# Performance work log

Hardware: AMD Instinct MI355X
Metric: run time of the kernel (lower is better)

Reference implementation:

```python
import jax, jax.numpy as jnp
import numpy as np

# Irreps structure (hardcoded per init_kwargs):
#  input  = 16x0e + 8x1o  -> dim 16 + 8*3 = 40
#  query  = key = 8x0e + 4x1o -> dim 8 + 4*3 = 20
#  output = 16x0e + 8x1o -> dim 40
#  edge_sh = 1x0e + 1x1o -> dim 4
M0, M1 = 16, 8          # input multiplicities (scalar, vector)
Q0, Q1 = 8, 4           # query/key multiplicities
O0, O1 = 16, 8          # output multiplicities
TPK_NUMEL = M0*Q0 + M1*Q0 + M0*Q1 + M1*Q1 + M1*Q1   # 320
TPV_NUMEL = M0*O0 + M1*O0 + M0*O1 + M1*O1 + M1*O1   # 640
EDGE_BASIS = 16
HIDDEN = 32


def _split(x):
    """Split irreps vector [*, m0 + 3*m1] into scalars [*, m0] and vectors [*, m1, 3]."""
    m0 = x.shape[-1] - 3 * ((x.shape[-1] - M0) // 3) if False else None
    return x  # placeholder, not used


def fc_net(x, w1, w2):
    """e3nn FullyConnectedNet: no biases, 1/sqrt(fan_in) scaling, silu hidden act."""
    h = jax.nn.silu((x @ w1) * (1.0 / np.sqrt(x.shape[-1])))
    return (h @ w2) * (1.0 / np.sqrt(w1.shape[-1]))


def fctp_edge(xs, xv, shs, shv, w, o0, o1):
    """FullyConnectedTensorProduct((m0x0e+m1x1o) x (1x0e+1x1o) -> (o0x0e+o1x1o))
    with per-edge weights w [E, numel]. Component-normalized CG, path-normalized output.
    xs:[E,m0] xv:[E,m1,3] shs:[E,1] shv:[E,3]."""
    m0, m1 = xs.shape[1], xv.shape[1]
    sizes = [m0*o0, m1*o0, m0*o1, m1*o1, m1*o1]
    offs = np.cumsum([0] + sizes)
    w1 = w[:, offs[0]:offs[1]].reshape(-1, m0, o0)
    w2 = w[:, offs[1]:offs[2]].reshape(-1, m1, o0)
    w3 = w[:, offs[2]:offs[3]].reshape(-1, m0, o1)
    w4 = w[:, offs[3]:offs[4]].reshape(-1, m1, o1)
    w5 = w[:, offs[4]:offs[5]].reshape(-1, m1, o1)
    # scalar output paths: 0e x 0e -> 0e ; 1o x 1o -> 0e (dot / sqrt3)
    p_ss = xs * shs                                            # [E,m0]
    p_vv = jnp.einsum('eic,ec->ei', xv, shv) * (1.0/np.sqrt(3.0))  # [E,m1]
    out_s = (jnp.einsum('ei,eio->eo', p_ss, w1)
             + jnp.einsum('ei,eio->eo', p_vv, w2)) * (1.0/np.sqrt(m0 + m1))
    # vector output paths: 0e x 1o ; 1o x 0e ; 1o x 1o -> 1o (cross / sqrt2)
    p_sv = xs[:, :, None] * shv[:, None, :]                    # [E,m0,3]
    p_vs = xv * shs[:, :, None]                                # [E,m1,3]
    p_xx = jnp.cross(xv, shv[:, None, :]) * (1.0/np.sqrt(2.0)) # [E,m1,3]
    out_v = (jnp.einsum('eic,eio->eoc', p_sv, w3)
             + jnp.einsum('eic,eio->eoc', p_vs, w4)
             + jnp.einsum('eic,eio->eoc', p_xx, w5)) * (1.0/np.sqrt(m0 + 2*m1))
    return out_s, out_v


def setup_inputs() -> dict:
    key = jax.random.key(0)
    ks = jax.random.split(key, 12)
    N, E = 10000, 100000
    node_ft = jax.random.normal(ks[0], (N, M0 + 3*M1), dtype=jnp.float32)
    edge_index = jax.random.randint(ks[1], (2, E), 0, N, dtype=jnp.int64)
    edge_sh = jax.random.normal(ks[2], (E, 4), dtype=jnp.float32)
    edge_scalars = jax.random.uniform(ks[3], (E, EDGE_BASIS), dtype=jnp.float32)
    # learned parameters
    w_q_s = jax.random.normal(ks[4], (M0, Q0), dtype=jnp.float32)
    w_q_v = jax.random.normal(ks[5], (M1, Q1), dtype=jnp.float32)
    fck_w1 = jax.random.normal(ks[6], (EDGE_BASIS, HIDDEN), dtype=jnp.float32)
    fck_w2 = jax.random.normal(ks[7], (HIDDEN, TPK_NUMEL), dtype=jnp.float32)
    fcv_w1 = jax.random.normal(ks[8], (EDGE_BASIS, HIDDEN), dtype=jnp.float32)
    fcv_w2 = jax.random.normal(ks[9], (HIDDEN, TPV_NUMEL), dtype=jnp.float32)
    wdot_s = jax.random.normal(ks[10], (Q0, Q0), dtype=jnp.float32)
    wdot_v = jax.random.normal(ks[11], (Q1, Q1), dtype=jnp.float32)
    return dict(node_ft=node_ft, edge_index=edge_index, edge_sh=edge_sh,
                edge_scalars=edge_scalars, w_q_s=w_q_s, w_q_v=w_q_v,
                fck_w1=fck_w1, fck_w2=fck_w2, fcv_w1=fcv_w1, fcv_w2=fcv_w2,
                wdot_s=wdot_s, wdot_v=wdot_v)


def reference(node_ft, edge_index, edge_sh, edge_scalars, w_q_s, w_q_v,
              fck_w1, fck_w2, fcv_w1, fcv_w2, wdot_s, wdot_v):
    N = node_ft.shape[0]
    sender, receiver = edge_index[0], edge_index[1]
    x_s = node_ft[:, :M0]                       # [N,16]
    x_v = node_ft[:, M0:].reshape(N, M1, 3)     # [N,8,3]
    # q = o3.Linear(input -> query): per-irrep linear mixing, 1/sqrt(mul) norm
    q_s = (x_s @ w_q_s) * (1.0/np.sqrt(M0))                    # [N,Q0]
    q_v = jnp.einsum('nic,io->noc', x_v, w_q_v) * (1.0/np.sqrt(M1))  # [N,Q1,3]
    sh_s, sh_v = edge_sh[:, :1], edge_sh[:, 1:4]
    xs_e, xv_e = x_s[sender], x_v[sender]       # gather sender features
    # per-edge tensor-product weights from radial MLPs
    wk = fc_net(edge_scalars, fck_w1, fck_w2)   # [E, 320]
    wv = fc_net(edge_scalars, fcv_w1, fcv_w2)   # [E, 640]
    k_s, k_v = fctp_edge(xs_e, xv_e, sh_s, sh_v, wk, Q0, Q1)
    v_s, v_v = fctp_edge(xs_e, xv_e, sh_s, sh_v, wv, O0, O1)
    # dot = FCTP(query, key -> 0e) with shared internal weights
    qr_s, qr_v = q_s[receiver], q_v[receiver]
    fan = Q0*Q0 + Q1*Q1
    dot = (jnp.einsum('ei,ej,ij->e', qr_s, k_s, wdot_s)
           + jnp.einsum('eic,ejc,ij->e', qr_v, k_v, wdot_v) * (1.0/np.sqrt(3.0))
           ) * (1.0/np.sqrt(fan))               # [E]
    # scatter-softmax over receiver
    ex = jnp.exp(dot)
    z = jax.ops.segment_sum(ex, receiver, num_segments=N)      # [N]
    alpha = ex / z[receiver]
    a = jnp.sqrt(jax.nn.relu(alpha))            # [E]
    out_s = jax.ops.segment_sum(a[:, None] * v_s, receiver, num_segments=N)
    out_v = jax.ops.segment_sum(a[:, None, None] * v_v, receiver, num_segments=N)
    return jnp.concatenate([out_s, out_v.reshape(N, O1*3)], axis=-1)  # [N,40]
```

## Files before the change

kernel.cpp:

```cpp
#include <hip/hip_runtime.h>


#define BS 256
#define EPB 64

typedef _Float16 half2_t __attribute__((ext_vector_type(2)));

#ifdef __has_builtin
#if __has_builtin(__builtin_amdgcn_fdot2)
#define USE_FDOT2 1
#endif
#endif

__device__ __forceinline__ float silu_f(float x) {
    return x * (1.0f / (1.0f + __expf(-x)));
}
__device__ __forceinline__ unsigned short f2h(float f) {
    return __builtin_bit_cast(unsigned short, (_Float16)f);
}
__device__ __forceinline__ unsigned pk2h(float a, float b) {
    return (unsigned)f2h(a) | ((unsigned)f2h(b) << 16);
}
__device__ __forceinline__ half2_t uh2(unsigned u) {
    return __builtin_bit_cast(half2_t, u);
}
__device__ __forceinline__ float d2(unsigned a, unsigned b, float c) {
#ifdef USE_FDOT2
    return __builtin_amdgcn_fdot2(uh2(a), uh2(b), c, false);
#else
    const half2_t ha = uh2(a), hb = uh2(b);
    return c + (float)ha[0] * (float)hb[0] + (float)ha[1] * (float)hb[1];
#endif
}
__device__ __forceinline__ float wred4(float v) {
    v += __shfl_xor(v, 16);
    v += __shfl_xor(v, 32);
    return v;
}

__global__ __launch_bounds__(256) void node_pre(
    const float* __restrict__ node_ft,
    const int*   __restrict__ ei,
    const float* __restrict__ w_q_s, const float* __restrict__ w_q_v,
    const float* __restrict__ wdot_s, const float* __restrict__ wdot_v,
    float* __restrict__ qd, int* __restrict__ cnt, int* __restrict__ flag,
    int N, int E)
{
    const int n = blockIdx.x * blockDim.x + threadIdx.x;
    if (n == 0) {
        int acc = 0;
        const int kmax = (E < 64) ? E : 64;
        for (int k = 0; k < kmax; ++k) acc |= ei[2*k + 1];
        *flag = (acc == 0) ? 1 : 0;
    }
    if (n >= N) return;
    cnt[n] = 0;

    const float* nf = node_ft + (size_t)n * 40;
    float xs[16];
#pragma unroll
    for (int i = 0; i < 16; ++i) xs[i] = nf[i];
    float q[8];
#pragma unroll
    for (int o = 0; o < 8; ++o) {
        float a = 0.f;
#pragma unroll
        for (int i = 0; i < 16; ++i) a += xs[i] * w_q_s[i*8 + o];
        q[o] = a * 0.25f;
    }
    float* qdn = qd + (size_t)n * 20;
#pragma unroll
    for (int j = 0; j < 8; ++j) {
        float a = 0.f;
#pragma unroll
        for (int i = 0; i < 8; ++i) a += q[i] * wdot_s[i*8 + j];
        qdn[j] = a;
    }
    float xv[8][3];
#pragma unroll
    for (int i = 0; i < 8; ++i)
#pragma unroll
        for (int c = 0; c < 3; ++c) xv[i][c] = nf[16 + i*3 + c];
    float qv[4][3];
#pragma unroll
    for (int o = 0; o < 4; ++o)
#pragma unroll
        for (int c = 0; c < 3; ++c) {
            float a = 0.f;
#pragma unroll
            for (int i = 0; i < 8; ++i) a += xv[i][c] * w_q_v[i*4 + o];
            qv[o][c] = a * 0.35355339059327379f;
        }
#pragma unroll
    for (int j = 0; j < 4; ++j)
#pragma unroll
        for (int c = 0; c < 3; ++c) {
            float a = 0.f;
#pragma unroll
            for (int i = 0; i < 4; ++i) a += qv[i][c] * wdot_v[i*4 + j];
            qdn[8 + j*3 + c] = a;
        }
}

__global__ __launch_bounds__(256) void count_edges(
    const int* __restrict__ ei, int* __restrict__ cnt,
    const int* __restrict__ flag, int E)
{
    const int e = blockIdx.x * blockDim.x + threadIdx.x;
    if (e >= E) return;
    const int is64 = *flag;
    const int rcv = is64 ? ei[2*(E + e)] : ei[E + e];
    atomicAdd(cnt + rcv, 1);
}

__global__ __launch_bounds__(1024) void scan_kernel(
    const int* __restrict__ cnt, int* __restrict__ start,
    int* __restrict__ cursor, int N)
{
    __shared__ int wsum[16];
    __shared__ int s_carry;
    const int tid = threadIdx.x, wave = tid >> 6, lane = tid & 63;
    if (tid == 0) s_carry = 0;
    __syncthreads();
    for (int base = 0; base < N; base += 1024) {
        const int i = base + tid;
        const int v = (i < N) ? cnt[i] : 0;
        int x = v;
#pragma unroll
        for (int d = 1; d < 64; d <<= 1) {
            const int y = __shfl_up(x, d, 64);
            if (lane >= d) x += y;
        }
        if (lane == 63) wsum[wave] = x;
        __syncthreads();
        if (wave == 0 && lane < 16) {
            int w = wsum[lane];
#pragma unroll
            for (int d = 1; d < 16; d <<= 1) {
                const int y = __shfl_up(w, d, 64);
                if (lane >= d) w += y;
            }
            wsum[lane] = w;
        }
        __syncthreads();
        const int woff = (wave == 0) ? 0 : wsum[wave - 1];
        const int carry = s_carry;
        if (i < N) {
            const int s = carry + woff + x - v;
            start[i] = s;
            cursor[i] = s;
        }
        __syncthreads();
        if (tid == 0) s_carry = carry + wsum[15];
        __syncthreads();
    }
    if (tid == 0) start[N] = s_carry;
}

__global__ __launch_bounds__(BS) void edge_k(
    const float* __restrict__ node_ft,
    const int*   __restrict__ ei,
    const float* __restrict__ edge_sh,
    const float* __restrict__ edge_scalars,
    const float* __restrict__ fck_w1,
    const float* __restrict__ fck_w2,
    const float* __restrict__ qd,
    int*   __restrict__ cursor,
    float* __restrict__ exbuf,
    float* __restrict__ sabuf,
    int*   __restrict__ posbuf,
    const int* __restrict__ flag,
    int N, int E)
{
    __shared__ uint4 sk4[4 * 321];

    const int tid = threadIdx.x;
    for (int idx = tid; idx < 4 * 320; idx += BS) {
        const int p = idx / 320;
        const int local = idx - p * 320;
        unsigned r0, r1, r2, r3;
        if (local < 128) {
            const int j = local >> 2, rr = local & 3, ip = rr >> 1, h = rr & 1;
            const int i0 = 4*p + 2*ip;
            const float* s0 = fck_w2 + j*320 + i0*8 + 4*h;
            const float* s1 = s0 + 8;
            r0 = pk2h(s0[0], s1[0]); r1 = pk2h(s0[1], s1[1]);
            r2 = pk2h(s0[2], s1[2]); r3 = pk2h(s0[3], s1[3]);
        } else if (local < 192) {
            const int l = local - 128; const int j = l >> 1, ip = l & 1;
            const int i0 = 4*p + 2*ip;
            const float* s0 = fck_w2 + j*320 + 192 + i0*4;
            const float* s1 = s0 + 4;
            r0 = pk2h(s0[0], s1[0]); r1 = pk2h(s0[1], s1[1]);
            r2 = pk2h(s0[2], s1[2]); r3 = pk2h(s0[3], s1[3]);
        } else if (local < 256) {
            const int l = local - 192; const int j = l >> 1, h = l & 1;
            const int i0 = 2*p;
            const float* s0 = fck_w2 + j*320 + 128 + i0*8 + 4*h;
            const float* s1 = s0 + 8;
            r0 = pk2h(s0[0], s1[0]); r1 = pk2h(s0[1], s1[1]);
            r2 = pk2h(s0[2], s1[2]); r3 = pk2h(s0[3], s1[3]);
        } else {
            const int l = local - 256; const int jp = l >> 2, rr = l & 3;
            const int il = rr >> 1, h = rr & 1;
            const int i = 2*p + il, j0 = 2*jp;
            const int col = (h == 0 ? 256 : 288) + i*4;
            const float* s0 = fck_w2 + j0*320 + col;
            const float* s1 = s0 + 320;
            r0 = pk2h(s0[0], s1[0]); r1 = pk2h(s0[1], s1[1]);
            r2 = pk2h(s0[2], s1[2]); r3 = pk2h(s0[3], s1[3]);
        }
        sk4[p * 321 + local] = make_uint4(r0, r1, r2, r3);
    }

    const int lane = tid & 63;
    const int p = lane >> 4;
    const int q = lane & 15;
    const int w = tid >> 6;
    const int e = blockIdx.x * EPB + w * 16 + q;
    const bool val = (e < E);
    const int ec = val ? e : (E - 1);

    const int is64 = *flag;
    const int snd = is64 ? ei[2*ec]       : ei[ec];
    const int rcv = is64 ? ei[2*(E + ec)] : ei[E + ec];

    int pos = 0;
    if (p == 0 && val) pos = atomicAdd(cursor + rcv, 1);

    const float4 s4 = *(const float4*)(edge_sh + (size_t)ec * 4);
    const float sh_s = s4.x;
    const float sh_v[3] = {s4.y, s4.z, s4.w};

    const float* nf = node_ft + (size_t)snd * 40;

    __syncthreads();

    float hk[32];
    {
        float es[16];
        const float4* a0 = (const float4*)(edge_scalars + (size_t)ec * 16);
#pragma unroll
        for (int t = 0; t < 4; ++t) {
            const float4 v = a0[t];
            es[4*t+0]=v.x; es[4*t+1]=v.y; es[4*t+2]=v.z; es[4*t+3]=v.w;
        }
#pragma unroll 8
        for (int j = 0; j < 32; ++j) {
            float a = 0.f;
#pragma unroll
            for (int t = 0; t < 16; ++t) a += es[t] * fck_w1[t*32 + j];
            hk[j] = silu_f(a * 0.25f);
        }
    }

    const uint4* g = sk4 + p * 321;

    const unsigned xs01 = pk2h(nf[4*p + 0], nf[4*p + 1]);
    const unsigned xs23 = pk2h(nf[4*p + 2], nf[4*p + 3]);

    float K1[8] = {};
#pragma unroll 8
    for (int j = 0; j < 32; ++j) {
        const uint4 A = g[j*4+0], B = g[j*4+1], C = g[j*4+2], D = g[j*4+3];
        const float h = hk[j];
        float t;
        t = d2(xs01, A.x, 0.f); t = d2(xs23, C.x, t); K1[0] += h*t;
        t = d2(xs01, A.y, 0.f); t = d2(xs23, C.y, t); K1[1] += h*t;
        t = d2(xs01, A.z, 0.f); t = d2(xs23, C.z, t); K1[2] += h*t;
        t = d2(xs01, A.w, 0.f); t = d2(xs23, C.w, t); K1[3] += h*t;
        t = d2(xs01, B.x, 0.f); t = d2(xs23, D.x, t); K1[4] += h*t;
        t = d2(xs01, B.y, 0.f); t = d2(xs23, D.y, t); K1[5] += h*t;
        t = d2(xs01, B.z, 0.f); t = d2(xs23, D.z, t); K1[6] += h*t;
        t = d2(xs01, B.w, 0.f); t = d2(xs23, D.w, t); K1[7] += h*t;
    }

    float K3[4] = {};
#pragma unroll 8
    for (int j = 0; j < 32; ++j) {
        const uint4 Ea = g[128 + j*2], Fb = g[128 + j*2 + 1];
        const float h = hk[j];
        float t;
        t = d2(xs01, Ea.x, 0.f); t = d2(xs23, Fb.x, t); K3[0] += h*t;
        t = d2(xs01, Ea.y, 0.f); t = d2(xs23, Fb.y, t); K3[1] += h*t;
        t = d2(xs01, Ea.z, 0.f); t = d2(xs23, Fb.z, t); K3[2] += h*t;
        t = d2(xs01, Ea.w, 0.f); t = d2(xs23, Fb.w, t); K3[3] += h*t;
    }

    const float c3 = 0.57735026918962576f;
    const float xa0 = nf[16 + 6*p], xa1 = nf[17 + 6*p], xa2 = nf[18 + 6*p];
    const float xb0 = nf[19 + 6*p], xb1 = nf[20 + 6*p], xb2 = nf[21 + 6*p];
    const float pv0 = (xa0*sh_v[0] + xa1*sh_v[1] + xa2*sh_v[2]) * c3;
    const float pv1 = (xb0*sh_v[0] + xb1*sh_v[1] + xb2*sh_v[2]) * c3;
    const unsigned pvp = pk2h(pv0, pv1);
    float K2[8] = {};
#pragma unroll 8
    for (int j = 0; j < 32; ++j) {
        const uint4 U = g[192 + j*2], V = g[192 + j*2 + 1];
        const float h = hk[j];
        K2[0] += h * d2(pvp, U.x, 0.f);
        K2[1] += h * d2(pvp, U.y, 0.f);
        K2[2] += h * d2(pvp, U.z, 0.f);
        K2[3] += h * d2(pvp, U.w, 0.f);
        K2[4] += h * d2(pvp, V.x, 0.f);
        K2[5] += h * d2(pvp, V.y, 0.f);
        K2[6] += h * d2(pvp, V.z, 0.f);
        K2[7] += h * d2(pvp, V.w, 0.f);
    }

    float W40[4] = {}, W41[4] = {}, W50[4] = {}, W51[4] = {};
#pragma unroll 4
    for (int jp = 0; jp < 16; ++jp) {
        const unsigned hp = pk2h(hk[2*jp], hk[2*jp+1]);
        const uint4 a = g[256 + jp*4 + 0];
        const uint4 b = g[256 + jp*4 + 1];
        const uint4 c = g[256 + jp*4 + 2];
        const uint4 d = g[256 + jp*4 + 3];
        W40[0] = d2(hp, a.x, W40[0]); W40[1] = d2(hp, a.y, W40[1]);
        W40[2] = d2(hp, a.z, W40[2]); W40[3] = d2(hp, a.w, W40[3]);
        W50[0] = d2(hp, b.x, W50[0]); W50[1] = d2(hp, b.y, W50[1]);
        W50[2] = d2(hp, b.z, W50[2]); W50[3] = d2(hp, b.w, W50[3]);
        W41[0] = d2(hp, c.x, W41[0]); W41[1] = d2(hp, c.y, W41[1]);
        W41[2] = d2(hp, c.z, W41[2]); W41[3] = d2(hp, c.w, W41[3]);
        W51[0] = d2(hp, d.x, W51[0]); W51[1] = d2(hp, d.y, W51[1]);
        W51[2] = d2(hp, d.z, W51[2]); W51[3] = d2(hp, d.w, W51[3]);
    }

    const float c7 = 0.70710678118654752f;
    float KV[12] = {};
    {
        const float s0 = sh_s*xa0, s1 = sh_s*xa1, s2 = sh_s*xa2;
        const float cx0 = c7*(xa1*sh_v[2] - xa2*sh_v[1]);
        const float cx1 = c7*(xa2*sh_v[0] - xa0*sh_v[2]);
        const float cx2 = c7*(xa0*sh_v[1] - xa1*sh_v[0]);
#pragma unroll
        for (int o = 0; o < 4; ++o) {
            KV[o*3+0] += s0*W40[o] + cx0*W50[o];
            KV[o*3+1] += s1*W40[o] + cx1*W50[o];
            KV[o*3+2] += s2*W40[o] + cx2*W50[o];
        }
    }
    {
        const float s0 = sh_s*xb0, s1 = sh_s*xb1, s2 = sh_s*xb2;
        const float cx0 = c7*(xb1*sh_v[2] - xb2*sh_v[1]);
        const float cx1 = c7*(xb2*sh_v[0] - xb0*sh_v[2]);
        const float cx2 = c7*(xb0*sh_v[1] - xb1*sh_v[0]);
#pragma unroll
        for (int o = 0; o < 4; ++o) {
            KV[o*3+0] += s0*W41[o] + cx0*W51[o];
            KV[o*3+1] += s1*W41[o] + cx1*W51[o];
            KV[o*3+2] += s2*W41[o] + cx2*W51[o];
        }
    }

#pragma unroll
    for (int o = 0; o < 8; ++o) K1[o] = wred4(K1[o]);
#pragma unroll
    for (int o = 0; o < 8; ++o) K2[o] = wred4(K2[o]);
#pragma unroll
    for (int o = 0; o < 4; ++o) K3[o] = wred4(K3[o]);
#pragma unroll
    for (int o = 0; o < 12; ++o) KV[o] = wred4(KV[o]);

    if (p == 0 && val) {
        float qdr[20];
        {
            const float4* rp = (const float4*)(qd + (size_t)rcv * 20);
#pragma unroll
            for (int t = 0; t < 5; ++t) {
                const float4 a = rp[t];
                qdr[4*t+0]=a.x; qdr[4*t+1]=a.y; qdr[4*t+2]=a.z; qdr[4*t+3]=a.w;
            }
        }
        float ds = 0.f;
#pragma unroll
        for (int o = 0; o < 8; ++o) ds += qdr[o] * (sh_s*K1[o] + K2[o]);
        float dv = 0.f;
#pragma unroll
        for (int o = 0; o < 4; ++o)
#pragma unroll
            for (int c = 0; c < 3; ++c)
                dv += qdr[8 + o*3 + c] * (K3[o]*sh_v[c] + KV[o*3+c]);
        const float dot = ds * 4.0343567508008e-3f + dv * 2.0171788261497e-3f;
        const float sa = __expf(0.5f * dot);
        exbuf[pos] = sa*sa; sabuf[e] = sa; posbuf[e] = pos;
    }
}

__global__ __launch_bounds__(BS) void edge_v_a(
    const float* __restrict__ node_ft,
    const int*   __restrict__ ei,
    const float* __restrict__ edge_sh,
    const float* __restrict__ edge_scalars,
    const float* __restrict__ fcv_w1,
    const float* __restrict__ fcv_w2,
    const float* __restrict__ sabuf,
    const int*   __restrict__ posbuf,
    float* __restrict__ vbuf,
    const int* __restrict__ flag,
    int E)
{
    __shared__ uint4 sa4[4 * 385];

    const int tid = threadIdx.x;
    for (int idx = tid; idx < 4 * 384; idx += BS) {
        const int p = idx / 384;
        const int local = idx - p * 384;
        const float* s0;
        const float* s1;
        if (local < 256) {
            const int j = local >> 3, rr = local & 7, ip = rr >> 2, h = rr & 3;
            const int i0 = 4*p + 2*ip;
            s0 = fcv_w2 + j*640 + i0*16 + h*4;
            s1 = s0 + 16;
        } else {
            const int l = local - 256; const int j = l >> 2, h = l & 3;
            const int i0 = 2*p;
            s0 = fcv_w2 + j*640 + 256 + i0*16 + h*4;
            s1 = s0 + 16;
        }
        sa4[p * 385 + local] = make_uint4(
            pk2h(s0[0], s1[0]), pk2h(s0[1], s1[1]),
            pk2h(s0[2], s1[2]), pk2h(s0[3], s1[3]));
    }

    const int lane = tid & 63;
    const int p = lane >> 4;
    const int q = lane & 15;
    const int w = tid >> 6;
    const int e = blockIdx.x * EPB + w * 16 + q;
    const bool val = (e < E);
    const int ec = val ? e : (E - 1);

    const int is64 = *flag;
    const int snd = is64 ? ei[2*ec] : ei[ec];

    const float4 s4 = *(const float4*)(edge_sh + (size_t)ec * 4);
    const float sh_s = s4.x;

    const float* nf = node_ft + (size_t)snd * 40;

    __syncthreads();

    float hv[32];
    {
        float es[16];
        const float4* a0 = (const float4*)(edge_scalars + (size_t)ec * 16);
#pragma unroll
        for (int t = 0; t < 4; ++t) {
            const float4 v = a0[t];
            es[4*t+0]=v.x; es[4*t+1]=v.y; es[4*t+2]=v.z; es[4*t+3]=v.w;
        }
#pragma unroll 8
        for (int j = 0; j < 32; ++j) {
            float a = 0.f;
#pragma unroll
            for (int t = 0; t < 16; ++t) a += es[t] * fcv_w1[t*32 + j];
            hv[j] = silu_f(a * 0.25f);
        }
    }

    const uint4* g = sa4 + p * 385;

    const unsigned xs01 = pk2h(nf[4*p + 0]*sh_s, nf[4*p + 1]*sh_s);
    const unsigned xs23 = pk2h(nf[4*p + 2]*sh_s, nf[4*p + 3]*sh_s);
    const float c3 = 0.57735026918962576f;
    const float pv0 = (nf[16+6*p]*s4.y + nf[17+6*p]*s4.z + nf[18+6*p]*s4.w) * c3;
    const float pv1 = (nf[19+6*p]*s4.y + nf[20+6*p]*s4.z + nf[21+6*p]*s4.w) * c3;
    const unsigned pvp = pk2h(pv0, pv1);

    float A[16] = {};

#pragma unroll 2
    for (int j = 0; j < 32; ++j) {
        const uint4* gw = g + j*8;
        const uint4 a0 = gw[0], a1 = gw[1], a2 = gw[2], a3 = gw[3];
        const uint4 b0 = gw[4], b1 = gw[5], b2 = gw[6], b3 = gw[7];
        const float h = hv[j];
        float t;
        t = d2(xs01, a0.x, 0.f); t = d2(xs23, b0.x, t); A[0]  += h*t;
        t = d2(xs01, a0.y, 0.f); t = d2(xs23, b0.y, t); A[1]  += h*t;
        t = d2(xs01, a0.z, 0.f); t = d2(xs23, b0.z, t); A[2]  += h*t;
        t = d2(xs01, a0.w, 0.f); t = d2(xs23, b0.w, t); A[3]  += h*t;
        t = d2(xs01, a1.x, 0.f); t = d2(xs23, b1.x, t); A[4]  += h*t;
        t = d2(xs01, a1.y, 0.f); t = d2(xs23, b1.y, t); A[5]  += h*t;
        t = d2(xs01, a1.z, 0.f); t = d2(xs23, b1.z, t); A[6]  += h*t;
        t = d2(xs01, a1.w, 0.f); t = d2(xs23, b1.w, t); A[7]  += h*t;
        t = d2(xs01, a2.x, 0.f); t = d2(xs23, b2.x, t); A[8]  += h*t;
        t = d2(xs01, a2.y, 0.f); t = d2(xs23, b2.y, t); A[9]  += h*t;
        t = d2(xs01, a2.z, 0.f); t = d2(xs23, b2.z, t); A[10] += h*t;
        t = d2(xs01, a2.w, 0.f); t = d2(xs23, b2.w, t); A[11] += h*t;
        t = d2(xs01, a3.x, 0.f); t = d2(xs23, b3.x, t); A[12] += h*t;
        t = d2(xs01, a3.y, 0.f); t = d2(xs23, b3.y, t); A[13] += h*t;
        t = d2(xs01, a3.z, 0.f); t = d2(xs23, b3.z, t); A[14] += h*t;
        t = d2(xs01, a3.w, 0.f); t = d2(xs23, b3.w, t); A[15] += h*t;
    }

#pragma unroll 4
    for (int j = 0; j < 32; ++j) {
        const uint4* gw = g + 256 + j*4;
        const uint4 u0 = gw[0], u1 = gw[1], u2 = gw[2], u3 = gw[3];
        const float h = hv[j];
        A[0]  += h * d2(pvp, u0.x, 0.f);
        A[1]  += h * d2(pvp, u0.y, 0.f);
        A[2]  += h * d2(pvp, u0.z, 0.f);
        A[3]  += h * d2(pvp, u0.w, 0.f);
        A[4]  += h * d2(pvp, u1.x, 0.f);
        A[5]  += h * d2(pvp, u1.y, 0.f);
        A[6]  += h * d2(pvp, u1.z, 0.f);
        A[7]  += h * d2(pvp, u1.w, 0.f);
        A[8]  += h * d2(pvp, u2.x, 0.f);
        A[9]  += h * d2(pvp, u2.y, 0.f);
        A[10] += h * d2(pvp, u2.z, 0.f);
        A[11] += h * d2(pvp, u2.w, 0.f);
        A[12] += h * d2(pvp, u3.x, 0.f);
        A[13] += h * d2(pvp, u3.y, 0.f);
        A[14] += h * d2(pvp, u3.z, 0.f);
        A[15] += h * d2(pvp, u3.w, 0.f);
    }

#pragma unroll
    for (int o = 0; o < 16; ++o) A[o] = wred4(A[o]);

    if (p == 0 && val) {
        const float cs = 0.03608439182435161f;
        const float sa = sabuf[e];
        const int pos = posbuf[e];
        float4* vp = (float4*)(vbuf + (size_t)pos * 40);
#pragma unroll
        for (int t = 0; t < 4; ++t) {
            float4 r;
            r.x = sa * A[4*t+0] * cs; r.y = sa * A[4*t+1] * cs;
            r.z = sa * A[4*t+2] * cs; r.w = sa * A[4*t+3] * cs;
            vp[t] = r;
        }
    }
}

__global__ __launch_bounds__(BS) void edge_v_b(
    const float* __restrict__ node_ft,
    const int*   __restrict__ ei,
    const float* __restrict__ edge_sh,
    const float* __restrict__ edge_scalars,
    const float* __restrict__ fcv_w1,
    const float* __restrict__ fcv_w2,
    const float* __restrict__ sabuf,
    const int*   __restrict__ posbuf,
    float* __restrict__ vbuf,
    const int* __restrict__ flag,
    int E)
{
    __shared__ uint4 sb4[4 * 257];

    const int tid = threadIdx.x;
    for (int idx = tid; idx < 4 * 256; idx += BS) {
        const int p = idx >> 8;
        const int local = idx & 255;
        const float* s0;
        const float* s1;
        if (local < 128) {
            const int j = local >> 2, rr = local & 3, ip = rr >> 1, h = rr & 1;
            const int i0 = 4*p + 2*ip;
            s0 = fcv_w2 + j*640 + 384 + i0*8 + 4*h;
            s1 = s0 + 8;
        } else {
            const int l = local - 128;
            const int jp = l >> 3, rr = l & 7, il = rr >> 2, h2 = rr & 3;
            const int i = 2*p + il, j0 = 2*jp;
            const int base = (h2 < 2) ? 512 : 576;
            s0 = fcv_w2 + j0*640 + base + i*8 + (h2 & 1)*4;
            s1 = s0 + 640;
        }
        sb4[p * 257 + local] = make_uint4(
            pk2h(s0[0], s1[0]), pk2h(s0[1], s1[1]),
            pk2h(s0[2], s1[2]), pk2h(s0[3], s1[3]));
    }

    const int lane = tid & 63;
    const int p = lane >> 4;
    const int q = lane & 15;
    const int w = tid >> 6;
    const int e = blockIdx.x * EPB + w * 16 + q;
    const bool val = (e < E);
    const int ec = val ? e : (E - 1);

    const int is64 = *flag;
    const int snd = is64 ? ei[2*ec] : ei[ec];

    const float4 s4 = *(const float4*)(edge_sh + (size_t)ec * 4);
    const float sh_s = s4.x;
    const float sh_v[3] = {s4.y, s4.z, s4.w};

    const float* nf = node_ft + (size_t)snd * 40;

    __syncthreads();

    float hv[32];
    {
        float es[16];
        const float4* a0 = (const float4*)(edge_scalars + (size_t)ec * 16);
#pragma unroll
        for (int t = 0; t < 4; ++t) {
            const float4 v = a0[t];
            es[4*t+0]=v.x; es[4*t+1]=v.y; es[4*t+2]=v.z; es[4*t+3]=v.w;
        }
#pragma unroll 8
        for (int j = 0; j < 32; ++j) {
            float a = 0.f;
#pragma unroll
            for (int t = 0; t < 16; ++t) a += es[t] * fcv_w1[t*32 + j];
            hv[j] = silu_f(a * 0.25f);
        }
    }

    const uint4* g = sb4 + p * 257;

    const unsigned xs01 = pk2h(nf[4*p + 0], nf[4*p + 1]);
    const unsigned xs23 = pk2h(nf[4*p + 2], nf[4*p + 3]);

    float T3[8] = {};
#pragma unroll 4
    for (int j = 0; j < 32; ++j) {
        const uint4 E0 = g[j*4+0], E1 = g[j*4+1];
        const uint4 F0 = g[j*4+2], F1 = g[j*4+3];
        const float h = hv[j];
        float t;
        t = d2(xs01, E0.x, 0.f); t = d2(xs23, F0.x, t); T3[0] += h*t;
        t = d2(xs01, E0.y, 0.f); t = d2(xs23, F0.y, t); T3[1] += h*t;
        t = d2(xs01, E0.z, 0.f); t = d2(xs23, F0.z, t); T3[2] += h*t;
        t = d2(xs01, E0.w, 0.f); t = d2(xs23, F0.w, t); T3[3] += h*t;
        t = d2(xs01, E1.x, 0.f); t = d2(xs23, F1.x, t); T3[4] += h*t;
        t = d2(xs01, E1.y, 0.f); t = d2(xs23, F1.y, t); T3[5] += h*t;
        t = d2(xs01, E1.z, 0.f); t = d2(xs23, F1.z, t); T3[6] += h*t;
        t = d2(xs01, E1.w, 0.f); t = d2(xs23, F1.w, t); T3[7] += h*t;
    }

    float W40[8] = {}, W41[8] = {}, W50[8] = {}, W51[8] = {};
#pragma unroll 2
    for (int jp = 0; jp < 16; ++jp) {
        const unsigned hp = pk2h(hv[2*jp], hv[2*jp+1]);
        const uint4* gw = g + 128 + jp*8;
        const uint4 a = gw[0], b = gw[1], c = gw[2], d = gw[3];
        const uint4 e2 = gw[4], f = gw[5], m = gw[6], n = gw[7];
        W40[0] = d2(hp, a.x, W40[0]); W40[1] = d2(hp, a.y, W40[1]);
        W40[2] = d2(hp, a.z, W40[2]); W40[3] = d2(hp, a.w, W40[3]);
        W40[4] = d2(hp, b.x, W40[4]); W40[5] = d2(hp, b.y, W40[5]);
        W40[6] = d2(hp, b.z, W40[6]); W40[7] = d2(hp, b.w, W40[7]);
        W50[0] = d2(hp, c.x, W50[0]); W50[1] = d2(hp, c.y, W50[1]);
        W50[2] = d2(hp, c.z, W50[2]); W50[3] = d2(hp, c.w, W50[3]);
        W50[4] = d2(hp, d.x, W50[4]); W50[5] = d2(hp, d.y, W50[5]);
        W50[6] = d2(hp, d.z, W50[6]); W50[7] = d2(hp, d.w, W50[7]);
        W41[0] = d2(hp, e2.x, W41[0]); W41[1] = d2(hp, e2.y, W41[1]);
        W41[2] = d2(hp, e2.z, W41[2]); W41[3] = d2(hp, e2.w, W41[3]);
        W41[4] = d2(hp, f.x, W41[4]); W41[5] = d2(hp, f.y, W41[5]);
        W41[6] = d2(hp, f.z, W41[6]); W41[7] = d2(hp, f.w, W41[7]);
        W51[0] = d2(hp, m.x, W51[0]); W51[1] = d2(hp, m.y, W51[1]);
        W51[2] = d2(hp, m.z, W51[2]); W51[3] = d2(hp, m.w, W51[3]);
        W51[4] = d2(hp, n.x, W51[4]); W51[5] = d2(hp, n.y, W51[5]);
        W51[6] = d2(hp, n.z, W51[6]); W51[7] = d2(hp, n.w, W51[7]);
    }

    const float c7 = 0.70710678118654752f;
    float R[24] = {};
    {
        const float x0 = nf[16 + 6*p], x1 = nf[17 + 6*p], x2 = nf[18 + 6*p];
        const float s0 = sh_s*x0, s1 = sh_s*x1, s2 = sh_s*x2;
        const float cx0 = c7*(x1*sh_v[2] - x2*sh_v[1]);
        const float cx1 = c7*(x2*sh_v[0] - x0*sh_v[2]);
        const float cx2 = c7*(x0*sh_v[1] - x1*sh_v[0]);
#pragma unroll
        for (int o = 0; o < 8; ++o) {
            R[o*3+0] += s0*W40[o] + cx0*W50[o];
            R[o*3+1] += s1*W40[o] + cx1*W50[o];
            R[o*3+2] += s2*W40[o] + cx2*W50[o];
        }
    }
    {
        const float x0 = nf[19 + 6*p], x1 = nf[20 + 6*p], x2 = nf[21 + 6*p];
        const float s0 = sh_s*x0, s1 = sh_s*x1, s2 = sh_s*x2;
        const float cx0 = c7*(x1*sh_v[2] - x2*sh_v[1]);
        const float cx1 = c7*(x2*sh_v[0] - x0*sh_v[2]);
        const float cx2 = c7*(x0*sh_v[1] - x1*sh_v[0]);
#pragma unroll
        for (int o = 0; o < 8; ++o) {
            R[o*3+0] += s0*W41[o] + cx0*W51[o];
            R[o*3+1] += s1*W41[o] + cx1*W51[o];
            R[o*3+2] += s2*W41[o] + cx2*W51[o];
        }
    }

#pragma unroll
    for (int o = 0; o < 8; ++o) T3[o] = wred4(T3[o]);
#pragma unroll
    for (int o = 0; o < 24; ++o) R[o] = wred4(R[o]);

    if (p == 0 && val) {
        const float sc = 0.03125f;
        const float sa = sabuf[e];
        const int pos = posbuf[e];
        float row[24];
#pragma unroll
        for (int o = 0; o < 8; ++o)
#pragma unroll
            for (int c = 0; c < 3; ++c)
                row[o*3+c] = sa * (T3[o]*sh_v[c] + R[o*3+c]) * sc;
        float4* vp = (float4*)(vbuf + (size_t)pos * 40 + 16);
#pragma unroll
        for (int t = 0; t < 6; ++t) {
            float4 r; r.x = row[4*t+0]; r.y = row[4*t+1]; r.z = row[4*t+2]; r.w = row[4*t+3];
            vp[t] = r;
        }
    }
}

__global__ __launch_bounds__(256) void node_reduce(
    const int*   __restrict__ start,
    const float* __restrict__ exbuf,
    const float* __restrict__ vbuf,
    float* __restrict__ out, int N)
{
    const int wave = threadIdx.x >> 6;
    const int lane = threadIdx.x & 63;
    const int n = blockIdx.x * 4 + wave;
    if (n >= N) return;
    const int r0 = start[n], r1 = start[n + 1];
    float z = 0.f, comp = 0.f;
    for (int r = r0; r < r1; ++r) {
        z += exbuf[r];
        if (lane < 40) comp += vbuf[(size_t)r * 40 + lane];
    }
    if (lane < 40)
        out[(size_t)n * 40 + lane] = (z > 0.f) ? comp * rsqrtf(z) : 0.f;
}

extern "C" void kernel_launch(void* const* d_in, const int* in_sizes, int n_in,
                              void* d_out, int out_size, void* d_ws, size_t ws_size,
                              hipStream_t stream) {
    const float* node_ft      = (const float*)d_in[0];
    const int*   edge_index   = (const int*)  d_in[1];
    const float* edge_sh      = (const float*)d_in[2];
    const float* edge_scalars = (const float*)d_in[3];
    const float* w_q_s        = (const float*)d_in[4];
    const float* w_q_v        = (const float*)d_in[5];
    const float* fck_w1       = (const float*)d_in[6];
    const float* fck_w2       = (const float*)d_in[7];
    const float* fcv_w1       = (const float*)d_in[8];
    const float* fcv_w2       = (const float*)d_in[9];
    const float* wdot_s       = (const float*)d_in[10];
    const float* wdot_v       = (const float*)d_in[11];

    const int N = in_sizes[0] / 40;
    const int E = in_sizes[2] / 4;

    float* ws    = (float*)d_ws;
    float* qd    = ws;
    int*   cnt   = (int*)(ws + (size_t)N * 20);
    int*   start = cnt + N;
    int*   curs  = start + N + 1;
    int*   flg   = curs + N;
    size_t off   = (size_t)N * 20 + N + (N + 1) + N + 1;
    off = (off + 3) & ~(size_t)3;
    float* exbuf  = ws + off;
    float* sabuf  = exbuf + E;
    int*   posbuf = (int*)(sabuf + E);
    float* vbuf   = (float*)(posbuf + E);

    float* out = (float*)d_out;

    const int EB = (E + EPB - 1) / EPB;

    hipLaunchKernelGGL(node_pre, dim3((N + 255) / 256), dim3(256), 0, stream,
                       node_ft, edge_index, w_q_s, w_q_v, wdot_s, wdot_v,
                       qd, cnt, flg, N, E);
    hipLaunchKernelGGL(count_edges, dim3((E + 255) / 256), dim3(256), 0, stream,
                       edge_index, cnt, flg, E);
    hipLaunchKernelGGL(scan_kernel, dim3(1), dim3(1024), 0, stream,
                       cnt, start, curs, N);
    hipLaunchKernelGGL(edge_k, dim3(EB), dim3(BS), 0, stream,
                       node_ft, edge_index, edge_sh, edge_scalars,
                       fck_w1, fck_w2, qd, curs, exbuf, sabuf, posbuf, flg, N, E);
    hipLaunchKernelGGL(edge_v_a, dim3(EB), dim3(BS), 0, stream,
                       node_ft, edge_index, edge_sh, edge_scalars,
                       fcv_w1, fcv_w2, sabuf, posbuf, vbuf, flg, E);
    hipLaunchKernelGGL(edge_v_b, dim3(EB), dim3(BS), 0, stream,
                       node_ft, edge_index, edge_sh, edge_scalars,
                       fcv_w1, fcv_w2, sabuf, posbuf, vbuf, flg, E);
    hipLaunchKernelGGL(node_reduce, dim3((N + 3) / 4), dim3(256), 0, stream,
                       start, exbuf, vbuf, out, N);
}
```

Before: 296.4 us.

## Process two edges per thread with packed fp16 FMA accumulation

Each thread now handles two edges, so the weights fetched from LDS once serve both, and the block size drops to 128 threads to keep 64 edges per block. The fdot2-based float accumulation is replaced by packed half-precision FMAs (v_pk_fma style) with fp16 accumulators that are summed to float only at the end. This aims to halve LDS traffic per edge and double arithmetic throughput. The cost is higher register pressure and lower accuracy, since accumulating in fp16 over 32 hidden units with round-toward-zero conversion can exceed the tolerance.

```diff
diff --git a/kernel.cpp b/kernel.cpp
--- a/kernel.cpp
+++ b/kernel.cpp
@@ -1,16 +1,10 @@
 #include <hip/hip_runtime.h>
 
 
-#define BS 256
+#define BS 128
 #define EPB 64
 
-typedef _Float16 half2_t __attribute__((ext_vector_type(2)));
-
-#ifdef __has_builtin
-#if __has_builtin(__builtin_amdgcn_fdot2)
-#define USE_FDOT2 1
-#endif
-#endif
+typedef _Float16 h2 __attribute__((ext_vector_type(2)));
 
 __device__ __forceinline__ float silu_f(float x) {
     return x * (1.0f / (1.0f + __expf(-x)));
@@ -21,17 +15,20 @@
 __device__ __forceinline__ unsigned pk2h(float a, float b) {
     return (unsigned)f2h(a) | ((unsigned)f2h(b) << 16);
 }
-__device__ __forceinline__ half2_t uh2(unsigned u) {
-    return __builtin_bit_cast(half2_t, u);
-}
-__device__ __forceinline__ float d2(unsigned a, unsigned b, float c) {
-#ifdef USE_FDOT2
-    return __builtin_amdgcn_fdot2(uh2(a), uh2(b), c, false);
-#else
-    const half2_t ha = uh2(a), hb = uh2(b);
-    return c + (float)ha[0] * (float)hb[0] + (float)ha[1] * (float)hb[1];
-#endif
-}
+__device__ __forceinline__ h2 uh2(unsigned u) {
+    return __builtin_bit_cast(h2, u);
+}
+__device__ __forceinline__ h2 pkrtz(float a, float b) {
+    return __builtin_bit_cast(h2, __builtin_amdgcn_cvt_pkrtz(a, b));
+}
+__device__ __forceinline__ h2 pfma(h2 a, h2 b, h2 c) {
+    return __builtin_elementwise_fma(a, b, c);
+}
+__device__ __forceinline__ float h2s(h2 a) {
+    return (float)a[0] + (float)a[1];
+}
+__device__ __forceinline__ h2 dup0(h2 a) { return __builtin_shufflevector(a, a, 0, 0); }
+__device__ __forceinline__ h2 dup1(h2 a) { return __builtin_shufflevector(a, a, 1, 1); }
 __device__ __forceinline__ float wred4(float v) {
     v += __shfl_xor(v, 16);
     v += __shfl_xor(v, 32);
@@ -217,173 +214,260 @@
     const int p = lane >> 4;
     const int q = lane & 15;
     const int w = tid >> 6;
-    const int e = blockIdx.x * EPB + w * 16 + q;
-    const bool val = (e < E);
-    const int ec = val ? e : (E - 1);
+    const int e0 = blockIdx.x * EPB + w * 32 + 2 * q;
+    const int e1 = e0 + 1;
+    const bool v0 = (e0 < E), v1 = (e1 < E);
+    const int e0c = v0 ? e0 : (E - 1);
+    const int e1c = v1 ? e1 : (E - 1);
 
     const int is64 = *flag;
-    const int snd = is64 ? ei[2*ec]       : ei[ec];
-    const int rcv = is64 ? ei[2*(E + ec)] : ei[E + ec];
-
-    int pos = 0;
-    if (p == 0 && val) pos = atomicAdd(cursor + rcv, 1);
-
-    const float4 s4 = *(const float4*)(edge_sh + (size_t)ec * 4);
-    const float sh_s = s4.x;
-    const float sh_v[3] = {s4.y, s4.z, s4.w};
-
-    const float* nf = node_ft + (size_t)snd * 40;
+    const int snd0 = is64 ? ei[2*e0c]       : ei[e0c];
+    const int rcv0 = is64 ? ei[2*(E + e0c)] : ei[E + e0c];
+    const int snd1 = is64 ? ei[2*e1c]       : ei[e1c];
+    const int rcv1 = is64 ? ei[2*(E + e1c)] : ei[E + e1c];
+
+    int pos0 = 0, pos1 = 0;
+    if (p == 0) {
+        if (v0) pos0 = atomicAdd(cursor + rcv0, 1);
+        if (v1) pos1 = atomicAdd(cursor + rcv1, 1);
+    }
+
+    const float4 s40 = *(const float4*)(edge_sh + (size_t)e0c * 4);
+    const float4 s41 = *(const float4*)(edge_sh + (size_t)e1c * 4);
+    const float sh_s0 = s40.x, sh_s1 = s41.x;
+    const float sh_v0[3] = {s40.y, s40.z, s40.w};
+    const float sh_v1[3] = {s41.y, s41.z, s41.w};
+
+    const float* nf0 = node_ft + (size_t)snd0 * 40;
+    const float* nf1 = node_ft + (size_t)snd1 * 40;
 
     __syncthreads();
 
-    float hk[32];
+    h2 hkp[32];
     {
-        float es[16];
-        const float4* a0 = (const float4*)(edge_scalars + (size_t)ec * 16);
+        float es0[16], es1[16];
+        const float4* a0 = (const float4*)(edge_scalars + (size_t)e0c * 16);
+        const float4* a1 = (const float4*)(edge_scalars + (size_t)e1c * 16);
 #pragma unroll
         for (int t = 0; t < 4; ++t) {
-            const float4 v = a0[t];
-            es[4*t+0]=v.x; es[4*t+1]=v.y; es[4*t+2]=v.z; es[4*t+3]=v.w;
+            const float4 a = a0[t], b = a1[t];
+            es0[4*t+0]=a.x; es0[4*t+1]=a.y; es0[4*t+2]=a.z; es0[4*t+3]=a.w;
+            es1[4*t+0]=b.x; es1[4*t+1]=b.y; es1[4*t+2]=b.z; es1[4*t+3]=b.w;
         }
 #pragma unroll 8
         for (int j = 0; j < 32; ++j) {
-            float a = 0.f;
-#pragma unroll
-            for (int t = 0; t < 16; ++t) a += es[t] * fck_w1[t*32 + j];
-            hk[j] = silu_f(a * 0.25f);
+            float a = 0.f, b = 0.f;
+#pragma unroll
+            for (int t = 0; t < 16; ++t) {
+                const float w1 = fck_w1[t*32 + j];
+                a += es0[t] * w1; b += es1[t] * w1;
+            }
+            hkp[j] = pkrtz(silu_f(a * 0.25f), silu_f(b * 0.25f));
         }
     }
 
     const uint4* g = sk4 + p * 321;
 
-    const unsigned xs01 = pk2h(nf[4*p + 0], nf[4*p + 1]);
-    const unsigned xs23 = pk2h(nf[4*p + 2], nf[4*p + 3]);
-
-    float K1[8] = {};
-#pragma unroll 8
+    const h2 xs01a = pkrtz(nf0[4*p + 0], nf0[4*p + 1]);
+    const h2 xs23a = pkrtz(nf0[4*p + 2], nf0[4*p + 3]);
+    const h2 xs01b = pkrtz(nf1[4*p + 0], nf1[4*p + 1]);
+    const h2 xs23b = pkrtz(nf1[4*p + 2], nf1[4*p + 3]);
+    const float c3 = 0.57735026918962576f;
+    const float xa00 = nf0[16 + 6*p], xa01 = nf0[17 + 6*p], xa02 = nf0[18 + 6*p];
+    const float xa10 = nf0[19 + 6*p], xa11 = nf0[20 + 6*p], xa12 = nf0[21 + 6*p];
+    const float xb00 = nf1[16 + 6*p], xb01 = nf1[17 + 6*p], xb02 = nf1[18 + 6*p];
+    const float xb10 = nf1[19 + 6*p], xb11 = nf1[20 + 6*p], xb12 = nf1[21 + 6*p];
+    const h2 pvpa = pkrtz((xa00*sh_v0[0] + xa01*sh_v0[1] + xa02*sh_v0[2]) * c3,
+                          (xa10*sh_v0[0] + xa11*sh_v0[1] + xa12*sh_v0[2]) * c3);
+    const h2 pvpb = pkrtz((xb00*sh_v1[0] + xb01*sh_v1[1] + xb02*sh_v1[2]) * c3,
+                          (xb10*sh_v1[0] + xb11*sh_v1[1] + xb12*sh_v1[2]) * c3);
+
+    h2 K1a[8] = {}, K3a[4] = {}, K2a[8] = {};
+    h2 K1b[8] = {}, K3b[4] = {}, K2b[8] = {};
+#pragma unroll 4
     for (int j = 0; j < 32; ++j) {
         const uint4 A = g[j*4+0], B = g[j*4+1], C = g[j*4+2], D = g[j*4+3];
-        const float h = hk[j];
-        float t;
-        t = d2(xs01, A.x, 0.f); t = d2(xs23, C.x, t); K1[0] += h*t;
-        t = d2(xs01, A.y, 0.f); t = d2(xs23, C.y, t); K1[1] += h*t;
-        t = d2(xs01, A.z, 0.f); t = d2(xs23, C.z, t); K1[2] += h*t;
-        t = d2(xs01, A.w, 0.f); t = d2(xs23, C.w, t); K1[3] += h*t;
-        t = d2(xs01, B.x, 0.f); t = d2(xs23, D.x, t); K1[4] += h*t;
-        t = d2(xs01, B.y, 0.f); t = d2(xs23, D.y, t); K1[5] += h*t;
-        t = d2(xs01, B.z, 0.f); t = d2(xs23, D.z, t); K1[6] += h*t;
-        t = d2(xs01, B.w, 0.f); t = d2(xs23, D.w, t); K1[7] += h*t;
-    }
-
-    float K3[4] = {};
-#pragma unroll 8
-    for (int j = 0; j < 32; ++j) {
         const uint4 Ea = g[128 + j*2], Fb = g[128 + j*2 + 1];
-        const float h = hk[j];
-        float t;
-        t = d2(xs01, Ea.x, 0.f); t = d2(xs23, Fb.x, t); K3[0] += h*t;
-        t = d2(xs01, Ea.y, 0.f); t = d2(xs23, Fb.y, t); K3[1] += h*t;
-        t = d2(xs01, Ea.z, 0.f); t = d2(xs23, Fb.z, t); K3[2] += h*t;
-        t = d2(xs01, Ea.w, 0.f); t = d2(xs23, Fb.w, t); K3[3] += h*t;
-    }
-
-    const float c3 = 0.57735026918962576f;
-    const float xa0 = nf[16 + 6*p], xa1 = nf[17 + 6*p], xa2 = nf[18 + 6*p];
-    const float xb0 = nf[19 + 6*p], xb1 = nf[20 + 6*p], xb2 = nf[21 + 6*p];
-    const float pv0 = (xa0*sh_v[0] + xa1*sh_v[1] + xa2*sh_v[2]) * c3;
-    const float pv1 = (xb0*sh_v[0] + xb1*sh_v[1] + xb2*sh_v[2]) * c3;
-    const unsigned pvp = pk2h(pv0, pv1);
-    float K2[8] = {};
-#pragma unroll 8
-    for (int j = 0; j < 32; ++j) {
         const uint4 U = g[192 + j*2], V = g[192 + j*2 + 1];
-        const float h = hk[j];
-        K2[0] += h * d2(pvp, U.x, 0.f);
-        K2[1] += h * d2(pvp, U.y, 0.f);
-        K2[2] += h * d2(pvp, U.z, 0.f);
-        K2[3] += h * d2(pvp, U.w, 0.f);
-        K2[4] += h * d2(pvp, V.x, 0.f);
-        K2[5] += h * d2(pvp, V.y, 0.f);
-        K2[6] += h * d2(pvp, V.z, 0.f);
-        K2[7] += h * d2(pvp, V.w, 0.f);
-    }
-
-    float W40[4] = {}, W41[4] = {}, W50[4] = {}, W51[4] = {};
+        const h2 hj = hkp[j];
+        {
+            const h2 hh = dup0(hj);
+            const h2 t01 = hh * xs01a, t23 = hh * xs23a, tp = hh * pvpa;
+            K1a[0]=pfma(t01,uh2(A.x),K1a[0]); K1a[0]=pfma(t23,uh2(C.x),K1a[0]);
+            K1a[1]=pfma(t01,uh2(A.y),K1a[1]); K1a[1]=pfma(t23,uh2(C.y),K1a[1]);
+            K1a[2]=pfma(t01,uh2(A.z),K1a[2]); K1a[2]=pfma(t23,uh2(C.z),K1a[2]);
+            K1a[3]=pfma(t01,uh2(A.w),K1a[3]); K1a[3]=pfma(t23,uh2(C.w),K1a[3]);
+            K1a[4]=pfma(t01,uh2(B.x),K1a[4]); K1a[4]=pfma(t23,uh2(D.x),K1a[4]);
+            K1a[5]=pfma(t01,uh2(B.y),K1a[5]); K1a[5]=pfma(t23,uh2(D.y),K1a[5]);
+            K1a[6]=pfma(t01,uh2(B.z),K1a[6]); K1a[6]=pfma(t23,uh2(D.z),K1a[6]);
+            K1a[7]=pfma(t01,uh2(B.w),K1a[7]); K1a[7]=pfma(t23,uh2(D.w),K1a[7]);
+            K3a[0]=pfma(t01,uh2(Ea.x),K3a[0]); K3a[0]=pfma(t23,uh2(Fb.x),K3a[0]);
+            K3a[1]=pfma(t01,uh2(Ea.y),K3a[1]); K3a[1]=pfma(t23,uh2(Fb.y),K3a[1]);
+            K3a[2]=pfma(t01,uh2(Ea.z),K3a[2]); K3a[2]=pfma(t23,uh2(Fb.z),K3a[2]);
+            K3a[3]=pfma(t01,uh2(Ea.w),K3a[3]); K3a[3]=pfma(t23,uh2(Fb.w),K3a[3]);
+            K2a[0]=pfma(tp,uh2(U.x),K2a[0]); K2a[1]=pfma(tp,uh2(U.y),K2a[1]);
+            K2a[2]=pfma(tp,uh2(U.z),K2a[2]); K2a[3]=pfma(tp,uh2(U.w),K2a[3]);
+            K2a[4]=pfma(tp,uh2(V.x),K2a[4]); K2a[5]=pfma(tp,uh2(V.y),K2a[5]);
+            K2a[6]=pfma(tp,uh2(V.z),K2a[6]); K2a[7]=pfma(tp,uh2(V.w),K2a[7]);
+        }
+        {
+            const h2 hh = dup1(hj);
+            const h2 t01 = hh * xs01b, t23 = hh * xs23b, tp = hh * pvpb;
+            K1b[0]=pfma(t01,uh2(A.x),K1b[0]); K1b[0]=pfma(t23,uh2(C.x),K1b[0]);
+            K1b[1]=pfma(t01,uh2(A.y),K1b[1]); K1b[1]=pfma(t23,uh2(C.y),K1b[1]);
+            K1b[2]=pfma(t01,uh2(A.z),K1b[2]); K1b[2]=pfma(t23,uh2(C.z),K1b[2]);
+            K1b[3]=pfma(t01,uh2(A.w),K1b[3]); K1b[3]=pfma(t23,uh2(C.w),K1b[3]);
+            K1b[4]=pfma(t01,uh2(B.x),K1b[4]); K1b[4]=pfma(t23,uh2(D.x),K1b[4]);
+            K1b[5]=pfma(t01,uh2(B.y),K1b[5]); K1b[5]=pfma(t23,uh2(D.y),K1b[5]);
+            K1b[6]=pfma(t01,uh2(B.z),K1b[6]); K1b[6]=pfma(t23,uh2(D.z),K1b[6]);
+            K1b[7]=pfma(t01,uh2(B.w),K1b[7]); K1b[7]=pfma(t23,uh2(D.w),K1b[7]);
+            K3b[0]=pfma(t01,uh2(Ea.x),K3b[0]); K3b[0]=pfma(t23,uh2(Fb.x),K3b[0]);
+            K3b[1]=pfma(t01,uh2(Ea.y),K3b[1]); K3b[1]=pfma(t23,uh2(Fb.y),K3b[1]);
+            K3b[2]=pfma(t01,uh2(Ea.z),K3b[2]); K3b[2]=pfma(t23,uh2(Fb.z),K3b[2]);
+            K3b[3]=pfma(t01,uh2(Ea.w),K3b[3]); K3b[3]=pfma(t23,uh2(Fb.w),K3b[3]);
+            K2b[0]=pfma(tp,uh2(U.x),K2b[0]); K2b[1]=pfma(tp,uh2(U.y),K2b[1]);
+            K2b[2]=pfma(tp,uh2(U.z),K2b[2]); K2b[3]=pfma(tp,uh2(U.w),K2b[3]);
+            K2b[4]=pfma(tp,uh2(V.x),K2b[4]); K2b[5]=pfma(tp,uh2(V.y),K2b[5]);
+            K2b[6]=pfma(tp,uh2(V.z),K2b[6]); K2b[7]=pfma(tp,uh2(V.w),K2b[7]);
+        }
+    }
+
+    h2 P4a[8] = {}, P5a[8] = {}, P4b[8] = {}, P5b[8] = {};
 #pragma unroll 4
     for (int jp = 0; jp < 16; ++jp) {
-        const unsigned hp = pk2h(hk[2*jp], hk[2*jp+1]);
-        const uint4 a = g[256 + jp*4 + 0];
-        const uint4 b = g[256 + jp*4 + 1];
-        const uint4 c = g[256 + jp*4 + 2];
-        const uint4 d = g[256 + jp*4 + 3];
-        W40[0] = d2(hp, a.x, W40[0]); W40[1] = d2(hp, a.y, W40[1]);
-        W40[2] = d2(hp, a.z, W40[2]); W40[3] = d2(hp, a.w, W40[3]);
-        W50[0] = d2(hp, b.x, W50[0]); W50[1] = d2(hp, b.y, W50[1]);
-        W50[2] = d2(hp, b.z, W50[2]); W50[3] = d2(hp, b.w, W50[3]);
-        W41[0] = d2(hp, c.x, W41[0]); W41[1] = d2(hp, c.y, W41[1]);
-        W41[2] = d2(hp, c.z, W41[2]); W41[3] = d2(hp, c.w, W41[3]);
-        W51[0] = d2(hp, d.x, W51[0]); W51[1] = d2(hp, d.y, W51[1]);
-        W51[2] = d2(hp, d.z, W51[2]); W51[3] = d2(hp, d.w, W51[3]);
+        const uint4 a4 = g[256 + jp*4 + 0];
+        const uint4 b4 = g[256 + jp*4 + 1];
+        const uint4 c4 = g[256 + jp*4 + 2];
+        const uint4 d4 = g[256 + jp*4 + 3];
+        const h2 hja = hkp[2*jp], hjb = hkp[2*jp+1];
+        const h2 hpa = __builtin_shufflevector(hja, hjb, 0, 2);
+        const h2 hpb = __builtin_shufflevector(hja, hjb, 1, 3);
+        P4a[0]=pfma(hpa,uh2(a4.x),P4a[0]); P4a[1]=pfma(hpa,uh2(a4.y),P4a[1]);
+        P4a[2]=pfma(hpa,uh2(a4.z),P4a[2]); P4a[3]=pfma(hpa,uh2(a4.w),P4a[3]);
+        P5a[0]=pfma(hpa,uh2(b4.x),P5a[0]); P5a[1]=pfma(hpa,uh2(b4.y),P5a[1]);
+        P5a[2]=pfma(hpa,uh2(b4.z),P5a[2]); P5a[3]=pfma(hpa,uh2(b4.w),P5a[3]);
+        P4a[4]=pfma(hpa,uh2(c4.x),P4a[4]); P4a[5]=pfma(hpa,uh2(c4.y),P4a[5]);
+        P4a[6]=pfma(hpa,uh2(c4.z),P4a[6]); P4a[7]=pfma(hpa,uh2(c4.w),P4a[7]);
+        P5a[4]=pfma(hpa,uh2(d4.x),P5a[4]); P5a[5]=pfma(hpa,uh2(d4.y),P5a[5]);
+        P5a[6]=pfma(hpa,uh2(d4.z),P5a[6]); P5a[7]=pfma(hpa,uh2(d4.w),P5a[7]);
+        P4b[0]=pfma(hpb,uh2(a4.x),P4b[0]); P4b[1]=pfma(hpb,uh2(a4.y),P4b[1]);
+        P4b[2]=pfma(hpb,uh2(a4.z),P4b[2]); P4b[3]=pfma(hpb,uh2(a4.w),P4b[3]);
+        P5b[0]=pfma(hpb,uh2(b4.x),P5b[0]); P5b[1]=pfma(hpb,uh2(b4.y),P5b[1]);
+        P5b[2]=pfma(hpb,uh2(b4.z),P5b[2]); P5b[3]=pfma(hpb,uh2(b4.w),P5b[3]);
+        P4b[4]=pfma(hpb,uh2(c4.x),P4b[4]); P4b[5]=pfma(hpb,uh2(c4.y),P4b[5]);
+        P4b[6]=pfma(hpb,uh2(c4.z),P4b[6]); P4b[7]=pfma(hpb,uh2(c4.w),P4b[7]);
+        P5b[4]=pfma(hpb,uh2(d4.x),P5b[4]); P5b[5]=pfma(hpb,uh2(d4.y),P5b[5]);
+        P5b[6]=pfma(hpb,uh2(d4.z),P5b[6]); P5b[7]=pfma(hpb,uh2(d4.w),P5b[7]);
     }
 
     const float c7 = 0.70710678118654752f;
-    float KV[12] = {};
+    float ds0 = 0.f, dv0 = 0.f, ds1 = 0.f, dv1 = 0.f;
     {
-        const float s0 = sh_s*xa0, s1 = sh_s*xa1, s2 = sh_s*xa2;
-        const float cx0 = c7*(xa1*sh_v[2] - xa2*sh_v[1]);
-        const float cx1 = c7*(xa2*sh_v[0] - xa0*sh_v[2]);
-        const float cx2 = c7*(xa0*sh_v[1] - xa1*sh_v[0]);
+        float qdr[20];
+        const float4* rp = (const float4*)(qd + (size_t)rcv0 * 20);
+#pragma unroll
+        for (int t = 0; t < 5; ++t) {
+            const float4 a = rp[t];
+            qdr[4*t+0]=a.x; qdr[4*t+1]=a.y; qdr[4*t+2]=a.z; qdr[4*t+3]=a.w;
+        }
+#pragma unroll
+        for (int o = 0; o < 8; ++o)
+            ds0 += qdr[o] * (sh_s0*h2s(K1a[o]) + h2s(K2a[o]));
+        float KV[12] = {};
+        {
+            const float s0=sh_s0*xa00, s1=sh_s0*xa01, s2=sh_s0*xa02;
+            const float cx0=c7*(xa01*sh_v0[2]-xa02*sh_v0[1]);
+            const float cx1=c7*(xa02*sh_v0[0]-xa00*sh_v0[2]);
+            const float cx2=c7*(xa00*sh_v0[1]-xa01*sh_v0[0]);
+#pragma unroll
+            for (int o = 0; o < 4; ++o) {
+                const float w4 = h2s(P4a[o]), w5 = h2s(P5a[o]);
+                KV[o*3+0] += s0*w4 + cx0*w5;
+                KV[o*3+1] += s1*w4 + cx1*w5;
+                KV[o*3+2] += s2*w4 + cx2*w5;
+            }
+        }
+        {
+            const float s0=sh_s0*xa10, s1=sh_s0*xa11, s2=sh_s0*xa12;
+            const float cx0=c7*(xa11*sh_v0[2]-xa12*sh_v0[1]);
+            const float cx1=c7*(xa12*sh_v0[0]-xa10*sh_v0[2]);
+            const float cx2=c7*(xa10*sh_v0[1]-xa11*sh_v0[0]);
+#pragma unroll
+            for (int o = 0; o < 4; ++o) {
+                const float w4 = h2s(P4a[4+o]), w5 = h2s(P5a[4+o]);
+                KV[o*3+0] += s0*w4 + cx0*w5;
+                KV[o*3+1] += s1*w4 + cx1*w5;
+                KV[o*3+2] += s2*w4 + cx2*w5;
+            }
+        }
 #pragma unroll
         for (int o = 0; o < 4; ++o) {
-            KV[o*3+0] += s0*W40[o] + cx0*W50[o];
-            KV[o*3+1] += s1*W40[o] + cx1*W50[o];
-            KV[o*3+2] += s2*W40[o] + cx2*W50[o];
+            const float k3 = h2s(K3a[o]);
+#pragma unroll
+            for (int c = 0; c < 3; ++c)
+                dv0 += qdr[8 + o*3 + c] * (k3*sh_v0[c] + KV[o*3+c]);
         }
     }
     {
-        const float s0 = sh_s*xb0, s1 = sh_s*xb1, s2 = sh_s*xb2;
-        const float cx0 = c7*(xb1*sh_v[2] - xb2*sh_v[1]);
-        const float cx1 = c7*(xb2*sh_v[0] - xb0*sh_v[2]);
-        const float cx2 = c7*(xb0*sh_v[1] - xb1*sh_v[0]);
+        float qdr[20];
+        const float4* rp = (const float4*)(qd + (size_t)rcv1 * 20);
+#pragma unroll
+        for (int t = 0; t < 5; ++t) {
+            const float4 a = rp[t];
+            qdr[4*t+0]=a.x; qdr[4*t+1]=a.y; qdr[4*t+2]=a.z; qdr[4*t+3]=a.w;
+        }
+#pragma unroll
+        for (int o = 0; o < 8; ++o)
+            ds1 += qdr[o] * (sh_s1*h2s(K1b[o]) + h2s(K2b[o]));
+        float KV[12] = {};
+        {
+            const float s0=sh_s1*xb00, s1=sh_s1*xb01, s2=sh_s1*xb02;
+            const float cx0=c7*(xb01*sh_v1[2]-xb02*sh_v1[1]);
+            const float cx1=c7*(xb02*sh_v1[0]-xb00*sh_v1[2]);
+            const float cx2=c7*(xb00*sh_v1[1]-xb01*sh_v1[0]);
+#pragma unroll
+            for (int o = 0; o < 4; ++o) {
+                const float w4 = h2s(P4b[o]), w5 = h2s(P5b[o]);
+                KV[o*3+0] += s0*w4 + cx0*w5;
+                KV[o*3+1] += s1*w4 + cx1*w5;
+                KV[o*3+2] += s2*w4 + cx2*w5;
+            }
+        }
+        {
+            const float s0=sh_s1*xb10, s1=sh_s1*xb11, s2=sh_s1*xb12;
+            const float cx0=c7*(xb11*sh_v1[2]-xb12*sh_v1[1]);
+            const float cx1=c7*(xb12*sh_v1[0]-xb10*sh_v1[2]);
+            const float cx2=c7*(xb10*sh_v1[1]-xb11*sh_v1[0]);
+#pragma unroll
+            for (int o = 0; o < 4; ++o) {
+                const float w4 = h2s(P4b[4+o]), w5 = h2s(P5b[4+o]);
+                KV[o*3+0] += s0*w4 + cx0*w5;
+                KV[o*3+1] += s1*w4 + cx1*w5;
+                KV[o*3+2] += s2*w4 + cx2*w5;
+            }
+        }
 #pragma unroll
         for (int o = 0; o < 4; ++o) {
-            KV[o*3+0] += s0*W41[o] + cx0*W51[o];
-            KV[o*3+1] += s1*W41[o] + cx1*W51[o];
-            KV[o*3+2] += s2*W41[o] + cx2*W51[o];
-        }
-    }
-
-#pragma unroll
-    for (int o = 0; o < 8; ++o) K1[o] = wred4(K1[o]);
-#pragma unroll
-    for (int o = 0; o < 8; ++o) K2[o] = wred4(K2[o]);
-#pragma unroll
-    for (int o = 0; o < 4; ++o) K3[o] = wred4(K3[o]);
-#pragma unroll
-    for (int o = 0; o < 12; ++o) KV[o] = wred4(KV[o]);
-
-    if (p == 0 && val) {
-        float qdr[20];
-        {
-            const float4* rp = (const float4*)(qd + (size_t)rcv * 20);
-#pragma unroll
-            for (int t = 0; t < 5; ++t) {
-                const float4 a = rp[t];
-                qdr[4*t+0]=a.x; qdr[4*t+1]=a.y; qdr[4*t+2]=a.z; qdr[4*t+3]=a.w;
-            }
-        }
-        float ds = 0.f;
-#pragma unroll
-        for (int o = 0; o < 8; ++o) ds += qdr[o] * (sh_s*K1[o] + K2[o]);
-        float dv = 0.f;
-#pragma unroll
-        for (int o = 0; o < 4; ++o)
+            const float k3 = h2s(K3b[o]);
 #pragma unroll
             for (int c = 0; c < 3; ++c)
-                dv += qdr[8 + o*3 + c] * (K3[o]*sh_v[c] + KV[o*3+c]);
-        const float dot = ds * 4.0343567508008e-3f + dv * 2.0171788261497e-3f;
-        const float sa = __expf(0.5f * dot);
-        exbuf[pos] = sa*sa; sabuf[e] = sa; posbuf[e] = pos;
+                dv1 += qdr[8 + o*3 + c] * (k3*sh_v1[c] + KV[o*3+c]);
+        }
+    }
+    ds0 = wred4(ds0); dv0 = wred4(dv0);
+    ds1 = wred4(ds1); dv1 = wred4(dv1);
+
+    if (p == 0) {
+        if (v0) {
+            const float dot = ds0 * 4.0343567508008e-3f + dv0 * 2.0171788261497e-3f;
+            const float sa = __expf(0.5f * dot);
+            exbuf[pos0] = sa*sa; sabuf[e0] = sa; posbuf[e0] = pos0;
+        }
+        if (v1) {
+            const float dot = ds1 * 4.0343567508008e-3f + dv1 * 2.0171788261497e-3f;
+            const float sa = __expf(0.5f * dot);
+            exbuf[pos1] = sa*sa; sabuf[e1] = sa; posbuf[e1] = pos1;
+        }
     }
 }
 
@@ -428,111 +512,141 @@
     const int p = lane >> 4;
     const int q = lane & 15;
     const int w = tid >> 6;
-    const int e = blockIdx.x * EPB + w * 16 + q;
-    const bool val = (e < E);
-    const int ec = val ? e : (E - 1);
+    const int e0 = blockIdx.x * EPB + w * 32 + 2 * q;
+    const int e1 = e0 + 1;
+    const bool v0 = (e0 < E), v1 = (e1 < E);
+    const int e0c = v0 ? e0 : (E - 1);
+    const int e1c = v1 ? e1 : (E - 1);
 
     const int is64 = *flag;
-    const int snd = is64 ? ei[2*ec] : ei[ec];
-
-    const float4 s4 = *(const float4*)(edge_sh + (size_t)ec * 4);
-    const float sh_s = s4.x;
-
-    const float* nf = node_ft + (size_t)snd * 40;
+    const int snd0 = is64 ? ei[2*e0c] : ei[e0c];
+    const int snd1 = is64 ? ei[2*e1c] : ei[e1c];
+
+    const float4 s40 = *(const float4*)(edge_sh + (size_t)e0c * 4);
+    const float4 s41 = *(const float4*)(edge_sh + (size_t)e1c * 4);
+
+    const float* nf0 = node_ft + (size_t)snd0 * 40;
+    const float* nf1 = node_ft + (size_t)snd1 * 40;
 
     __syncthreads();
 
-    float hv[32];
+    h2 hvp[32];
     {
-        float es[16];
-        const float4* a0 = (const float4*)(edge_scalars + (size_t)ec * 16);
+        float es0[16], es1[16];
+        const float4* a0 = (const float4*)(edge_scalars + (size_t)e0c * 16);
+        const float4* a1 = (const float4*)(edge_scalars + (size_t)e1c * 16);
 #pragma unroll
         for (int t = 0; t < 4; ++t) {
-            const float4 v = a0[t];
-            es[4*t+0]=v.x; es[4*t+1]=v.y; es[4*t+2]=v.z; es[4*t+3]=v.w;
+            const float4 a = a0[t], b = a1[t];
+            es0[4*t+0]=a.x; es0[4*t+1]=a.y; es0[4*t+2]=a.z; es0[4*t+3]=a.w;
+            es1[4*t+0]=b.x; es1[4*t+1]=b.y; es1[4*t+2]=b.z; es1[4*t+3]=b.w;
         }
 #pragma unroll 8
         for (int j = 0; j < 32; ++j) {
-            float a = 0.f;
-#pragma unroll
-            for (int t = 0; t < 16; ++t) a += es[t] * fcv_w1[t*32 + j];
-            hv[j] = silu_f(a * 0.25f);
+            float a = 0.f, b = 0.f;
+#pragma unroll
+            for (int t = 0; t < 16; ++t) {
+                const float w1 = fcv_w1[t*32 + j];
+                a += es0[t] * w1; b += es1[t] * w1;
+            }
+            hvp[j] = pkrtz(silu_f(a * 0.25f), silu_f(b * 0.25f));
         }
     }
 
     const uint4* g = sa4 + p * 385;
 
-    const unsigned xs01 = pk2h(nf[4*p + 0]*sh_s, nf[4*p + 1]*sh_s);
-    const unsigned xs23 = pk2h(nf[4*p + 2]*sh_s, nf[4*p + 3]*sh_s);
+    const h2 xs01a = pkrtz(nf0[4*p + 0]*s40.x, nf0[4*p + 1]*s40.x);
+    const h2 xs23a = pkrtz(nf0[4*p + 2]*s40.x, nf0[4*p + 3]*s40.x);
+    const h2 xs01b = pkrtz(nf1[4*p + 0]*s41.x, nf1[4*p + 1]*s41.x);
+    const h2 xs23b = pkrtz(nf1[4*p + 2]*s41.x, nf1[4*p + 3]*s41.x);
     const float c3 = 0.57735026918962576f;
-    const float pv0 = (nf[16+6*p]*s4.y + nf[17+6*p]*s4.z + nf[18+6*p]*s4.w) * c3;
-    const float pv1 = (nf[19+6*p]*s4.y + nf[20+6*p]*s4.z + nf[21+6*p]*s4.w) * c3;
-    const unsigned pvp = pk2h(pv0, pv1);
-
-    float A[16] = {};
-
+    const h2 pvpa = pkrtz(
+        (nf0[16+6*p]*s40.y + nf0[17+6*p]*s40.z + nf0[18+6*p]*s40.w) * c3,
+        (nf0[19+6*p]*s40.y + nf0[20+6*p]*s40.z + nf0[21+6*p]*s40.w) * c3);
+    const h2 pvpb = pkrtz(
+        (nf1[16+6*p]*s41.y + nf1[17+6*p]*s41.z + nf1[18+6*p]*s41.w) * c3,
+        (nf1[19+6*p]*s41.y + nf1[20+6*p]*s41.z + nf1[21+6*p]*s41.w) * c3);
+
+    h2 Aa[16] = {}, Ab[16] = {};
 #pragma unroll 2
     for (int j = 0; j < 32; ++j) {
         const uint4* gw = g + j*8;
         const uint4 a0 = gw[0], a1 = gw[1], a2 = gw[2], a3 = gw[3];
         const uint4 b0 = gw[4], b1 = gw[5], b2 = gw[6], b3 = gw[7];
-        const float h = hv[j];
-        float t;
-        t = d2(xs01, a0.x, 0.f); t = d2(xs23, b0.x, t); A[0]  += h*t;
-        t = d2(xs01, a0.y, 0.f); t = d2(xs23, b0.y, t); A[1]  += h*t;
-        t = d2(xs01, a0.z, 0.f); t = d2(xs23, b0.z, t); A[2]  += h*t;
-        t = d2(xs01, a0.w, 0.f); t = d2(xs23, b0.w, t); A[3]  += h*t;
-        t = d2(xs01, a1.x, 0.f); t = d2(xs23, b1.x, t); A[4]  += h*t;
-        t = d2(xs01, a1.y, 0.f); t = d2(xs23, b1.y, t); A[5]  += h*t;
-        t = d2(xs01, a1.z, 0.f); t = d2(xs23, b1.z, t); A[6]  += h*t;
-        t = d2(xs01, a1.w, 0.f); t = d2(xs23, b1.w, t); A[7]  += h*t;
-        t = d2(xs01, a2.x, 0.f); t = d2(xs23, b2.x, t); A[8]  += h*t;
-        t = d2(xs01, a2.y, 0.f); t = d2(xs23, b2.y, t); A[9]  += h*t;
-        t = d2(xs01, a2.z, 0.f); t = d2(xs23, b2.z, t); A[10] += h*t;
-        t = d2(xs01, a2.w, 0.f); t = d2(xs23, b2.w, t); A[11] += h*t;
-        t = d2(xs01, a3.x, 0.f); t = d2(xs23, b3.x, t); A[12] += h*t;
-        t = d2(xs01, a3.y, 0.f); t = d2(xs23, b3.y, t); A[13] += h*t;
-        t = d2(xs01, a3.z, 0.f); t = d2(xs23, b3.z, t); A[14] += h*t;
-        t = d2(xs01, a3.w, 0.f); t = d2(xs23, b3.w, t); A[15] += h*t;
-    }
-
-#pragma unroll 4
-    for (int j = 0; j < 32; ++j) {
-        const uint4* gw = g + 256 + j*4;
-        const uint4 u0 = gw[0], u1 = gw[1], u2 = gw[2], u3 = gw[3];
-        const float h = hv[j];
-        A[0]  += h * d2(pvp, u0.x, 0.f);
-        A[1]  += h * d2(pvp, u0.y, 0.f);
-        A[2]  += h * d2(pvp, u0.z, 0.f);
-        A[3]  += h * d2(pvp, u0.w, 0.f);
-        A[4]  += h * d2(pvp, u1.x, 0.f);
-        A[5]  += h * d2(pvp, u1.y, 0.f);
-        A[6]  += h * d2(pvp, u1.z, 0.f);
-        A[7]  += h * d2(pvp, u1.w, 0.f);
-        A[8]  += h * d2(pvp, u2.x, 0.f);
-        A[9]  += h * d2(pvp, u2.y, 0.f);
-        A[10] += h * d2(pvp, u2.z, 0.f);
-        A[11] += h * d2(pvp, u2.w, 0.f);
-        A[12] += h * d2(pvp, u3.x, 0.f);
-        A[13] += h * d2(pvp, u3.y, 0.f);
-        A[14] += h * d2(pvp, u3.z, 0.f);
-        A[15] += h * d2(pvp, u3.w, 0.f);
-    }
-
-#pragma unroll
-    for (int o = 0; o < 16; ++o) A[o] = wred4(A[o]);
-
-    if (p == 0 && val) {
+        const uint4* g2 = g + 256 + j*4;
+        const uint4 u0 = g2[0], u1 = g2[1], u2 = g2[2], u3 = g2[3];
+        const h2 hj = hvp[j];
+        {
+            const h2 hh = dup0(hj);
+            const h2 t01 = hh * xs01a, t23 = hh * xs23a, tp = hh * pvpa;
+            Aa[0] =pfma(t01,uh2(a0.x),Aa[0]);  Aa[0] =pfma(t23,uh2(b0.x),Aa[0]);  Aa[0] =pfma(tp,uh2(u0.x),Aa[0]);
+            Aa[1] =pfma(t01,uh2(a0.y),Aa[1]);  Aa[1] =pfma(t23,uh2(b0.y),Aa[1]);  Aa[1] =pfma(tp,uh2(u0.y),Aa[1]);
+            Aa[2] =pfma(t01,uh2(a0.z),Aa[2]);  Aa[2] =pfma(t23,uh2(b0.z),Aa[2]);  Aa[2] =pfma(tp,uh2(u0.z),Aa[2]);
+            Aa[3] =pfma(t01,uh2(a0.w),Aa[3]);  Aa[3] =pfma(t23,uh2(b0.w),Aa[3]);  Aa[3] =pfma(tp,uh2(u0.w),Aa[3]);
+            Aa[4] =pfma(t01,uh2(a1.x),Aa[4]);  Aa[4] =pfma(t23,uh2(b1.x),Aa[4]);  Aa[4] =pfma(tp,uh2(u1.x),Aa[4]);
+            Aa[5] =pfma(t01,uh2(a1.y),Aa[5]);  Aa[5] =pfma(t23,uh2(b1.y),Aa[5]);  Aa[5] =pfma(tp,uh2(u1.y),Aa[5]);
+            Aa[6] =pfma(t01,uh2(a1.z),Aa[6]);  Aa[6] =pfma(t23,uh2(b1.z),Aa[6]);  Aa[6] =pfma(tp,uh2(u1.z),Aa[6]);
+            Aa[7] =pfma(t01,uh2(a1.w),Aa[7]);  Aa[7] =pfma(t23,uh2(b1.w),Aa[7]);  Aa[7] =pfma(tp,uh2(u1.w),Aa[7]);
+            Aa[8] =pfma(t01,uh2(a2.x),Aa[8]);  Aa[8] =pfma(t23,uh2(b2.x),Aa[8]);  Aa[8] =pfma(tp,uh2(u2.x),Aa[8]);
+            Aa[9] =pfma(t01,uh2(a2.y),Aa[9]);  Aa[9] =pfma(t23,uh2(b2.y),Aa[9]);  Aa[9] =pfma(tp,uh2(u2.y),Aa[9]);
+            Aa[10]=pfma(t01,uh2(a2.z),Aa[10]); Aa[10]=pfma(t23,uh2(b2.z),Aa[10]); Aa[10]=pfma(tp,uh2(u2.z),Aa[10]);
+            Aa[11]=pfma(t01,uh2(a2.w),Aa[11]); Aa[11]=pfma(t23,uh2(b2.w),Aa[11]); Aa[11]=pfma(tp,uh2(u2.w),Aa[11]);
+            Aa[12]=pfma(t01,uh2(a3.x),Aa[12]); Aa[12]=pfma(t23,uh2(b3.x),Aa[12]); Aa[12]=pfma(tp,uh2(u3.x),Aa[12]);
+            Aa[13]=pfma(t01,uh2(a3.y),Aa[13]); Aa[13]=pfma(t23,uh2(b3.y),Aa[13]); Aa[13]=pfma(tp,uh2(u3.y),Aa[13]);
+            Aa[14]=pfma(t01,uh2(a3.z),Aa[14]); Aa[14]=pfma(t23,uh2(b3.z),Aa[14]); Aa[14]=pfma(tp,uh2(u3.z),Aa[14]);
+            Aa[15]=pfma(t01,uh2(a3.w),Aa[15]); Aa[15]=pfma(t23,uh2(b3.w),Aa[15]); Aa[15]=pfma(tp,uh2(u3.w),Aa[15]);
+        }
+        {
+            const h2 hh = dup1(hj);
+            const h2 t01 = hh * xs01b, t23 = hh * xs23b, tp = hh * pvpb;
+            Ab[0] =pfma(t01,uh2(a0.x),Ab[0]);  Ab[0] =pfma(t23,uh2(b0.x),Ab[0]);  Ab[0] =pfma(tp,uh2(u0.x),Ab[0]);
+            Ab[1] =pfma(t01,uh2(a0.y),Ab[1]);  Ab[1] =pfma(t23,uh2(b0.y),Ab[1]);  Ab[1] =pfma(tp,uh2(u0.y),Ab[1]);
+            Ab[2] =pfma(t01,uh2(a0.z),Ab[2]);  Ab[2] =pfma(t23,uh2(b0.z),Ab[2]);  Ab[2] =pfma(tp,uh2(u0.z),Ab[2]);
+            Ab[3] =pfma(t01,uh2(a0.w),Ab[3]);  Ab[3] =pfma(t23,uh2(b0.w),Ab[3]);  Ab[3] =pfma(tp,uh2(u0.w),Ab[3]);
+            Ab[4] =pfma(t01,uh2(a1.x),Ab[4]);  Ab[4] =pfma(t23,uh2(b1.x),Ab[4]);  Ab[4] =pfma(tp,uh2(u1.x),Ab[4]);
+            Ab[5] =pfma(t01,uh2(a1.y),Ab[5]);  Ab[5] =pfma(t23,uh2(b1.y),Ab[5]);  Ab[5] =pfma(tp,uh2(u1.y),Ab[5]);
+            Ab[6] =pfma(t01,uh2(a1.z),Ab[6]);  Ab[6] =pfma(t23,uh2(b1.z),Ab[6]);  Ab[6] =pfma(tp,uh2(u1.z),Ab[6]);
+            Ab[7] =pfma(t01,uh2(a1.w),Ab[7]);  Ab[7] =pfma(t23,uh2(b1.w),Ab[7]);  Ab[7] =pfma(tp,uh2(u1.w),Ab[7]);
+            Ab[8] =pfma(t01,uh2(a2.x),Ab[8]);  Ab[8] =pfma(t23,uh2(b2.x),Ab[8]);  Ab[8] =pfma(tp,uh2(u2.x),Ab[8]);
+            Ab[9] =pfma(t01,uh2(a2.y),Ab[9]);  Ab[9] =pfma(t23,uh2(b2.y),Ab[9]);  Ab[9] =pfma(tp,uh2(u2.y),Ab[9]);
+            Ab[10]=pfma(t01,uh2(a2.z),Ab[10]); Ab[10]=pfma(t23,uh2(b2.z),Ab[10]); Ab[10]=pfma(tp,uh2(u2.z),Ab[10]);
+            Ab[11]=pfma(t01,uh2(a2.w),Ab[11]); Ab[11]=pfma(t23,uh2(b2.w),Ab[11]); Ab[11]=pfma(tp,uh2(u2.w),Ab[11]);
+            Ab[12]=pfma(t01,uh2(a3.x),Ab[12]); Ab[12]=pfma(t23,uh2(b3.x),Ab[12]); Ab[12]=pfma(tp,uh2(u3.x),Ab[12]);
+            Ab[13]=pfma(t01,uh2(a3.y),Ab[13]); Ab[13]=pfma(t23,uh2(b3.y),Ab[13]); Ab[13]=pfma(tp,uh2(u3.y),Ab[13]);
+            Ab[14]=pfma(t01,uh2(a3.z),Ab[14]); Ab[14]=pfma(t23,uh2(b3.z),Ab[14]); Ab[14]=pfma(tp,uh2(u3.z),Ab[14]);
+            Ab[15]=pfma(t01,uh2(a3.w),Ab[15]); Ab[15]=pfma(t23,uh2(b3.w),Ab[15]); Ab[15]=pfma(tp,uh2(u3.w),Ab[15]);
+        }
+    }
+
+    float A0[16], A1[16];
+#pragma unroll
+    for (int o = 0; o < 16; ++o) { A0[o] = wred4(h2s(Aa[o])); A1[o] = wred4(h2s(Ab[o])); }
+
+    if (p == 0) {
         const float cs = 0.03608439182435161f;
-        const float sa = sabuf[e];
-        const int pos = posbuf[e];
-        float4* vp = (float4*)(vbuf + (size_t)pos * 40);
-#pragma unroll
-        for (int t = 0; t < 4; ++t) {
-            float4 r;
-            r.x = sa * A[4*t+0] * cs; r.y = sa * A[4*t+1] * cs;
-            r.z = sa * A[4*t+2] * cs; r.w = sa * A[4*t+3] * cs;
-            vp[t] = r;
+        if (v0) {
+            const float sa = sabuf[e0];
+            const int pos = posbuf[e0];
+            float4* vp = (float4*)(vbuf + (size_t)pos * 40);
+#pragma unroll
+            for (int t = 0; t < 4; ++t) {
+                float4 r;
+                r.x = sa * A0[4*t+0] * cs; r.y = sa * A0[4*t+1] * cs;
+                r.z = sa * A0[4*t+2] * cs; r.w = sa * A0[4*t+3] * cs;
+                vp[t] = r;
+            }
+        }
+        if (v1) {
+            const float sa = sabuf[e1];
+            const int pos = posbuf[e1];
+            float4* vp = (float4*)(vbuf + (size_t)pos * 40);
+#pragma unroll
+            for (int t = 0; t < 4; ++t) {
+                float4 r;
+                r.x = sa * A1[4*t+0] * cs; r.y = sa * A1[4*t+1] * cs;
+                r.z = sa * A1[4*t+2] * cs; r.w = sa * A1[4*t+3] * cs;
+                vp[t] = r;
+            }
         }
     }
 }
@@ -565,10 +679,10 @@
             s1 = s0 + 8;
         } else {
             const int l = local - 128;
-            const int jp = l >> 3, rr = l & 7, il = rr >> 2, h2 = rr & 3;
+            const int jp = l >> 3, rr = l & 7, il = rr >> 2, h2c = rr & 3;
             const int i = 2*p + il, j0 = 2*jp;
-            const int base = (h2 < 2) ? 512 : 576;
-            s0 = fcv_w2 + j0*640 + base + i*8 + (h2 & 1)*4;
+            const int base = (h2c < 2) ? 512 : 576;
+            s0 = fcv_w2 + j0*640 + base + i*8 + (h2c & 1)*4;
             s1 = s0 + 640;
         }
         sb4[p * 257 + local] = make_uint4(
@@ -580,135 +694,242 @@
     const int p = lane >> 4;
     const int q = lane & 15;
     const int w = tid >> 6;
-    const int e = blockIdx.x * EPB + w * 16 + q;
-    const bool val = (e < E);
-    const int ec = val ? e : (E - 1);
+    const int e0 = blockIdx.x * EPB + w * 32 + 2 * q;
+    const int e1 = e0 + 1;
+    const bool v0 = (e0 < E), v1 = (e1 < E);
+    const int e0c = v0 ? e0 : (E - 1);
+    const int e1c = v1 ? e1 : (E - 1);
 
     const int is64 = *flag;
-    const int snd = is64 ? ei[2*ec] : ei[ec];
-
-    const float4 s4 = *(const float4*)(edge_sh + (size_t)ec * 4);
-    const float sh_s = s4.x;
-    const float sh_v[3] = {s4.y, s4.z, s4.w};
-
-    const float* nf = node_ft + (size_t)snd * 40;
+    const int snd0 = is64 ? ei[2*e0c] : ei[e0c];
+    const int snd1 = is64 ? ei[2*e1c] : ei[e1c];
+
+    const float4 s40 = *(const float4*)(edge_sh + (size_t)e0c * 4);
+    const float4 s41 = *(const float4*)(edge_sh + (size_t)e1c * 4);
+    const float sh_s0 = s40.x, sh_s1 = s41.x;
+    const float sh_v0[3] = {s40.y, s40.z, s40.w};
+    const float sh_v1[3] = {s41.y, s41.z, s41.w};
+
+    const float* nf0 = node_ft + (size_t)snd0 * 40;
+    const float* nf1 = node_ft + (size_t)snd1 * 40;
 
     __syncthreads();
 
-    float hv[32];
+    h2 hvp[32];
     {
-        float es[16];
-        const float4* a0 = (const float4*)(edge_scalars + (size_t)ec * 16);
+        float es0[16], es1[16];
+        const float4* a0 = (const float4*)(edge_scalars + (size_t)e0c * 16);
+        const float4* a1 = (const float4*)(edge_scalars + (size_t)e1c * 16);
 #pragma unroll
         for (int t = 0; t < 4; ++t) {
-            const float4 v = a0[t];
-            es[4*t+0]=v.x; es[4*t+1]=v.y; es[4*t+2]=v.z; es[4*t+3]=v.w;
+            const float4 a = a0[t], b = a1[t];
+            es0[4*t+0]=a.x; es0[4*t+1]=a.y; es0[4*t+2]=a.z; es0[4*t+3]=a.w;
+            es1[4*t+0]=b.x; es1[4*t+1]=b.y; es1[4*t+2]=b.z; es1[4*t+3]=b.w;
         }
 #pragma unroll 8
         for (int j = 0; j < 32; ++j) {
-            float a = 0.f;
-#pragma unroll
-            for (int t = 0; t < 16; ++t) a += es[t] * fcv_w1[t*32 + j];
-            hv[j] = silu_f(a * 0.25f);
+            float a = 0.f, b = 0.f;
+#pragma unroll
+            for (int t = 0; t < 16; ++t) {
+                const float w1 = fcv_w1[t*32 + j];
+                a += es0[t] * w1; b += es1[t] * w1;
+            }
+            hvp[j] = pkrtz(silu_f(a * 0.25f), silu_f(b * 0.25f));
         }
     }
 
     const uint4* g = sb4 + p * 257;
 
-    const unsigned xs01 = pk2h(nf[4*p + 0], nf[4*p + 1]);
-    const unsigned xs23 = pk2h(nf[4*p + 2], nf[4*p + 3]);
-
-    float T3[8] = {};
+    const h2 xs01a = pkrtz(nf0[4*p + 0], nf0[4*p + 1]);
+    const h2 xs23a = pkrtz(nf0[4*p + 2], nf0[4*p + 3]);
+    const h2 xs01b = pkrtz(nf1[4*p + 0], nf1[4*p + 1]);
+    const h2 xs23b = pkrtz(nf1[4*p + 2], nf1[4*p + 3]);
+
+    h2 T3a[8] = {}, T3b[8] = {};
 #pragma unroll 4
     for (int j = 0; j < 32; ++j) {
         const uint4 E0 = g[j*4+0], E1 = g[j*4+1];
         const uint4 F0 = g[j*4+2], F1 = g[j*4+3];
-        const float h = hv[j];
-        float t;
-        t = d2(xs01, E0.x, 0.f); t = d2(xs23, F0.x, t); T3[0] += h*t;
-        t = d2(xs01, E0.y, 0.f); t = d2(xs23, F0.y, t); T3[1] += h*t;
-        t = d2(xs01, E0.z, 0.f); t = d2(xs23, F0.z, t); T3[2] += h*t;
-        t = d2(xs01, E0.w, 0.f); t = d2(xs23, F0.w, t); T3[3] += h*t;
-        t = d2(xs01, E1.x, 0.f); t = d2(xs23, F1.x, t); T3[4] += h*t;
-        t = d2(xs01, E1.y, 0.f); t = d2(xs23, F1.y, t); T3[5] += h*t;
-        t = d2(xs01, E1.z, 0.f); t = d2(xs23, F1.z, t); T3[6] += h*t;
-        t = d2(xs01, E1.w, 0.f); t = d2(xs23, F1.w, t); T3[7] += h*t;
-    }
-
-    float W40[8] = {}, W41[8] = {}, W50[8] = {}, W51[8] = {};
+        const h2 hj = hvp[j];
+        {
+            const h2 hh = dup0(hj);
+            const h2 t01 = hh * xs01a, t23 = hh * xs23a;
+            T3a[0]=pfma(t01,uh2(E0.x),T3a[0]); T3a[0]=pfma(t23,uh2(F0.x),T3a[0]);
+            T3a[1]=pfma(t01,uh2(E0.y),T3a[1]); T3a[1]=pfma(t23,uh2(F0.y),T3a[1]);
+            T3a[2]=pfma(t01,uh2(E0.z),T3a[2]); T3a[2]=pfma(t23,uh2(F0.z),T3a[2]);
+            T3a[3]=pfma(t01,uh2(E0.w),T3a[3]); T3a[3]=pfma(t23,uh2(F0.w),T3a[3]);
+            T3a[4]=pfma(t01,uh2(E1.x),T3a[4]); T3a[4]=pfma(t23,uh2(F1.x),T3a[4]);
+            T3a[5]=pfma(t01,uh2(E1.y),T3a[5]); T3a[5]=pfma(t23,uh2(F1.y),T3a[5]);
+            T3a[6]=pfma(t01,uh2(E1.z),T3a[6]); T3a[6]=pfma(t23,uh2(F1.z),T3a[6]);
+            T3a[7]=pfma(t01,uh2(E1.w),T3a[7]); T3a[7]=pfma(t23,uh2(F1.w),T3a[7]);
+        }
+        {
+            const h2 hh = dup1(hj);
+            const h2 t01 = hh * xs01b, t23 = hh * xs23b;
+            T3b[0]=pfma(t01,uh2(E0.x),T3b[0]); T3b[0]=pfma(t23,uh2(F0.x),T3b[0]);
+            T3b[1]=pfma(t01,uh2(E0.y),T3b[1]); T3b[1]=pfma(t23,uh2(F0.y),T3b[1]);
+            T3b[2]=pfma(t01,uh2(E0.z),T3b[2]); T3b[2]=pfma(t23,uh2(F0.z),T3b[2]);
+            T3b[3]=pfma(t01,uh2(E0.w),T3b[3]); T3b[3]=pfma(t23,uh2(F0.w),T3b[3]);
+            T3b[4]=pfma(t01,uh2(E1.x),T3b[4]); T3b[4]=pfma(t23,uh2(F1.x),T3b[4]);
+            T3b[5]=pfma(t01,uh2(E1.y),T3b[5]); T3b[5]=pfma(t23,uh2(F1.y),T3b[5]);
+            T3b[6]=pfma(t01,uh2(E1.z),T3b[6]); T3b[6]=pfma(t23,uh2(F1.z),T3b[6]);
+            T3b[7]=pfma(t01,uh2(E1.w),T3b[7]); T3b[7]=pfma(t23,uh2(F1.w),T3b[7]);
+        }
+    }
+
+    h2 P4a[16] = {}, P5a[16] = {}, P4b[16] = {}, P5b[16] = {};
 #pragma unroll 2
     for (int jp = 0; jp < 16; ++jp) {
-        const unsigned hp = pk2h(hv[2*jp], hv[2*jp+1]);
         const uint4* gw = g + 128 + jp*8;
-        const uint4 a = gw[0], b = gw[1], c = gw[2], d = gw[3];
-        const uint4 e2 = gw[4], f = gw[5], m = gw[6], n = gw[7];
-        W40[0] = d2(hp, a.x, W40[0]); W40[1] = d2(hp, a.y, W40[1]);
-        W40[2] = d2(hp, a.z, W40[2]); W40[3] = d2(hp, a.w, W40[3]);
-        W40[4] = d2(hp, b.x, W40[4]); W40[5] = d2(hp, b.y, W40[5]);
-        W40[6] = d2(hp, b.z, W40[6]); W40[7] = d2(hp, b.w, W40[7]);
-        W50[0] = d2(hp, c.x, W50[0]); W50[1] = d2(hp, c.y, W50[1]);
-        W50[2] = d2(hp, c.z, W50[2]); W50[3] = d2(hp, c.w, W50[3]);
-        W50[4] = d2(hp, d.x, W50[4]); W50[5] = d2(hp, d.y, W50[5]);
-        W50[6] = d2(hp, d.z, W50[6]); W50[7] = d2(hp, d.w, W50[7]);
-        W41[0] = d2(hp, e2.x, W41[0]); W41[1] = d2(hp, e2.y, W41[1]);
-        W41[2] = d2(hp, e2.z, W41[2]); W41[3] = d2(hp, e2.w, W41[3]);
-        W41[4] = d2(hp, f.x, W41[4]); W41[5] = d2(hp, f.y, W41[5]);
-        W41[6] = d2(hp, f.z, W41[6]); W41[7] = d2(hp, f.w, W41[7]);
-        W51[0] = d2(hp, m.x, W51[0]); W51[1] = d2(hp, m.y, W51[1]);
-        W51[2] = d2(hp, m.z, W51[2]); W51[3] = d2(hp, m.w, W51[3]);
-        W51[4] = d2(hp, n.x, W51[4]); W51[5] = d2(hp, n.y, W51[5]);
-        W51[6] = d2(hp, n.z, W51[6]); W51[7] = d2(hp, n.w, W51[7]);
+        const uint4 a4 = gw[0], b4 = gw[1];
+        const uint4 c4 = gw[2], d4 = gw[3];
+        const uint4 e4 = gw[4], f4 = gw[5];
+        const uint4 m4 = gw[6], n4 = gw[7];
+        const h2 hja = hvp[2*jp], hjb = hvp[2*jp+1];
+        const h2 hpa = __builtin_shufflevector(hja, hjb, 0, 2);
+        const h2 hpb = __builtin_shufflevector(hja, hjb, 1, 3);
+        P4a[0] =pfma(hpa,uh2(a4.x),P4a[0]);  P4a[1] =pfma(hpa,uh2(a4.y),P4a[1]);
+        P4a[2] =pfma(hpa,uh2(a4.z),P4a[2]);  P4a[3] =pfma(hpa,uh2(a4.w),P4a[3]);
+        P4a[4] =pfma(hpa,uh2(b4.x),P4a[4]);  P4a[5] =pfma(hpa,uh2(b4.y),P4a[5]);
+        P4a[6] =pfma(hpa,uh2(b4.z),P4a[6]);  P4a[7] =pfma(hpa,uh2(b4.w),P4a[7]);
+        P5a[0] =pfma(hpa,uh2(c4.x),P5a[0]);  P5a[1] =pfma(hpa,uh2(c4.y),P5a[1]);
+        P5a[2] =pfma(hpa,uh2(c4.z),P5a[2]);  P5a[3] =pfma(hpa,uh2(c4.w),P5a[3]);
+        P5a[4] =pfma(hpa,uh2(d4.x),P5a[4]);  P5a[5] =pfma(hpa,uh2(d4.y),P5a[5]);
+        P5a[6] =pfma(hpa,uh2(d4.z),P5a[6]);  P5a[7] =pfma(hpa,uh2(d4.w),P5a[7]);
+        P4a[8] =pfma(hpa,uh2(e4.x),P4a[8]);  P4a[9] =pfma(hpa,uh2(e4.y),P4a[9]);
+        P4a[10]=pfma(hpa,uh2(e4.z),P4a[10]); P4a[11]=pfma(hpa,uh2(e4.w),P4a[11]);
+        P4a[12]=pfma(hpa,uh2(f4.x),P4a[12]); P4a[13]=pfma(hpa,uh2(f4.y),P4a[13]);
+        P4a[14]=pfma(hpa,uh2(f4.z),P4a[14]); P4a[15]=pfma(hpa,uh2(f4.w),P4a[15]);
+        P5a[8] =pfma(hpa,uh2(m4.x),P5a[8]);  P5a[9] =pfma(hpa,uh2(m4.y),P5a[9]);
+        P5a[10]=pfma(hpa,uh2(m4.z),P5a[10]); P5a[11]=pfma(hpa,uh2(m4.w),P5a[11]);
+        P5a[12]=pfma(hpa,uh2(n4.x),P5a[12]); P5a[13]=pfma(hpa,uh2(n4.y),P5a[13]);
+        P5a[14]=pfma(hpa,uh2(n4.z),P5a[14]); P5a[15]=pfma(hpa,uh2(n4.w),P5a[15]);
+        P4b[0] =pfma(hpb,uh2(a4.x),P4b[0]);  P4b[1] =pfma(hpb,uh2(a4.y),P4b[1]);
+        P4b[2] =pfma(hpb,uh2(a4.z),P4b[2]);  P4b[3] =pfma(hpb,uh2(a4.w),P4b[3]);
+        P4b[4] =pfma(hpb,uh2(b4.x),P4b[4]);  P4b[5] =pfma(hpb,uh2(b4.y),P4b[5]);
+        P4b[6] =pfma(hpb,uh2(b4.z),P4b[6]);  P4b[7] =pfma(hpb,uh2(b4.w),P4b[7]);
+        P5b[0] =pfma(hpb,uh2(c4.x),P5b[0]);  P5b[1] =pfma(hpb,uh2(c4.y),P5b[1]);
+        P5b[2] =pfma(hpb,uh2(c4.z),P5b[2]);  P5b[3] =pfma(hpb,uh2(c4.w),P5b[3]);
+        P5b[4] =pfma(hpb,uh2(d4.x),P5b[4]);  P5b[5] =pfma(hpb,uh2(d4.y),P5b[5]);
+        P5b[6] =pfma(hpb,uh2(d4.z),P5b[6]);  P5b[7] =pfma(hpb,uh2(d4.w),P5b[7]);
+        P4b[8] =pfma(hpb,uh2(e4.x),P4b[8]);  P4b[9] =pfma(hpb,uh2(e4.y),P4b[9]);
+        P4b[10]=pfma(hpb,uh2(e4.z),P4b[10]); P4b[11]=pfma(hpb,uh2(e4.w),P4b[11]);
+        P4b[12]=pfma(hpb,uh2(f4.x),P4b[12]); P4b[13]=pfma(hpb,uh2(f4.y),P4b[13]);
+        P4b[14]=pfma(hpb,uh2(f4.z),P4b[14]); P4b[15]=pfma(hpb,uh2(f4.w),P4b[15]);
+        P5b[8] =pfma(hpb,uh2(m4.x),P5b[8]);  P5b[9] =pfma(hpb,uh2(m4.y),P5b[9]);
+        P5b[10]=pfma(hpb,uh2(m4.z),P5b[10]); P5b[11]=pfma(hpb,uh2(m4.w),P5b[11]);
+        P5b[12]=pfma(hpb,uh2(n4.x),P5b[12]); P5b[13]=pfma(hpb,uh2(n4.y),P5b[13]);
+        P5b[14]=pfma(hpb,uh2(n4.z),P5b[14]); P5b[15]=pfma(hpb,uh2(n4.w),P5b[15]);
     }
 
     const float c7 = 0.70710678118654752f;
-    float R[24] = {};
+    float R0[24], R1[24], T30[8], T31[8];
     {
-        const float x0 = nf[16 + 6*p], x1 = nf[17 + 6*p], x2 = nf[18 + 6*p];
-        const float s0 = sh_s*x0, s1 = sh_s*x1, s2 = sh_s*x2;
-        const float cx0 = c7*(x1*sh_v[2] - x2*sh_v[1]);
-        const float cx1 = c7*(x2*sh_v[0] - x0*sh_v[2]);
-        const float cx2 = c7*(x0*sh_v[1] - x1*sh_v[0]);
-#pragma unroll
-        for (int o = 0; o < 8; ++o) {
-            R[o*3+0] += s0*W40[o] + cx0*W50[o];
-            R[o*3+1] += s1*W40[o] + cx1*W50[o];
-            R[o*3+2] += s2*W40[o] + cx2*W50[o];
-        }
+        float acc[24];
+#pragma unroll
+        for (int o = 0; o < 24; ++o) acc[o] = 0.f;
+        {
+            const float x0 = nf0[16 + 6*p], x1 = nf0[17 + 6*p], x2 = nf0[18 + 6*p];
+            const float s0 = sh_s0*x0, s1 = sh_s0*x1, s2 = sh_s0*x2;
+            const float cx0 = c7*(x1*sh_v0[2] - x2*sh_v0[1]);
+            const float cx1 = c7*(x2*sh_v0[0] - x0*sh_v0[2]);
+            const float cx2 = c7*(x0*sh_v0[1] - x1*sh_v0[0]);
+#pragma unroll
+            for (int o = 0; o < 8; ++o) {
+                const float w4 = h2s(P4a[o]), w5 = h2s(P5a[o]);
+                acc[o*3+0] += s0*w4 + cx0*w5;
+                acc[o*3+1] += s1*w4 + cx1*w5;
+                acc[o*3+2] += s2*w4 + cx2*w5;
+            }
+        }
+        {
+            const float x0 = nf0[19 + 6*p], x1 = nf0[20 + 6*p], x2 = nf0[21 + 6*p];
+            const float s0 = sh_s0*x0, s1 = sh_s0*x1, s2 = sh_s0*x2;
+            const float cx0 = c7*(x1*sh_v0[2] - x2*sh_v0[1]);
+            const float cx1 = c7*(x2*sh_v0[0] - x0*sh_v0[2]);
+            const float cx2 = c7*(x0*sh_v0[1] - x1*sh_v0[0]);
+#pragma unroll
+            for (int o = 0; o < 8; ++o) {
+                const float w4 = h2s(P4a[8+o]), w5 = h2s(P5a[8+o]);
+                acc[o*3+0] += s0*w4 + cx0*w5;
+                acc[o*3+1] += s1*w4 + cx1*w5;
+                acc[o*3+2] += s2*w4 + cx2*w5;
+            }
+        }
+#pragma unroll
+        for (int o = 0; o < 24; ++o) R0[o] = wred4(acc[o]);
     }
     {
-        const float x0 = nf[19 + 6*p], x1 = nf[20 + 6*p], x2 = nf[21 + 6*p];
-        const float s0 = sh_s*x0, s1 = sh_s*x1, s2 = sh_s*x2;
-        const float cx0 = c7*(x1*sh_v[2] - x2*sh_v[1]);
-        const float cx1 = c7*(x2*sh_v[0] - x0*sh_v[2]);
-        const float cx2 = c7*(x0*sh_v[1] - x1*sh_v[0]);
-#pragma unroll
-        for (int o = 0; o < 8; ++o) {
-            R[o*3+0] += s0*W41[o] + cx0*W51[o];
-            R[o*3+1] += s1*W41[o] + cx1*W51[o];
-            R[o*3+2] += s2*W41[o] + cx2*W51[o];
-        }
-    }
-
-#pragma unroll
-    for (int o = 0; o < 8; ++o) T3[o] = wred4(T3[o]);
-#pragma unroll
-    for (int o = 0; o < 24; ++o) R[o] = wred4(R[o]);
-
-    if (p == 0 && val) {
+        float acc[24];
+#pragma unroll
+        for (int o = 0; o < 24; ++o) acc[o] = 0.f;
+        {
+            const float x0 = nf1[16 + 6*p], x1 = nf1[17 + 6*p], x2 = nf1[18 + 6*p];
+            const float s0 = sh_s1*x0, s1 = sh_s1*x1, s2 = sh_s1*x2;
+            const float cx0 = c7*(x1*sh_v1[2] - x2*sh_v1[1]);
+            const float cx1 = c7*(x2*sh_v1[0] - x0*sh_v1[2]);
+            const float cx2 = c7*(x0*sh_v1[1] - x1*sh_v1[0]);
+#pragma unroll
+            for (int o = 0; o < 8; ++o) {
+                const float w4 = h2s(P4b[o]), w5 = h2s(P5b[o]);
+                acc[o*3+0] += s0*w4 + cx0*w5;
+                acc[o*3+1] += s1*w4 + cx1*w5;
+                acc[o*3+2] += s2*w4 + cx2*w5;
+            }
+        }
+        {
+            const float x0 = nf1[19 + 6*p], x1 = nf1[20 + 6*p], x2 = nf1[21 + 6*p];
+            const float s0 = sh_s1*x0, s1 = sh_s1*x1, s2 = sh_s1*x2;
+            const float cx0 = c7*(x1*sh_v1[2] - x2*sh_v1[1]);
+            const float cx1 = c7*(x2*sh_v1[0] - x0*sh_v1[2]);
+            const float cx2 = c7*(x0*sh_v1[1] - x1*sh_v1[0]);
+#pragma unroll
+            for (int o = 0; o < 8; ++o) {
+                const float w4 = h2s(P4b[8+o]), w5 = h2s(P5b[8+o]);
+                acc[o*3+0] += s0*w4 + cx0*w5;
+                acc[o*3+1] += s1*w4 + cx1*w5;
+                acc[o*3+2] += s2*w4 + cx2*w5;
+            }
+        }
+#pragma unroll
+        for (int o = 0; o < 24; ++o) R1[o] = wred4(acc[o]);
+    }
+#pragma unroll
+    for (int o = 0; o < 8; ++o) { T30[o] = wred4(h2s(T3a[o])); T31[o] = wred4(h2s(T3b[o])); }
+
+    if (p == 0) {
         const float sc = 0.03125f;
-        const float sa = sabuf[e];
-        const int pos = posbuf[e];
-        float row[24];
-#pragma unroll
-        for (int o = 0; o < 8; ++o)
-#pragma unroll
-            for (int c = 0; c < 3; ++c)
-                row[o*3+c] = sa * (T3[o]*sh_v[c] + R[o*3+c]) * sc;
-        float4* vp = (float4*)(vbuf + (size_t)pos * 40 + 16);
-#pragma unroll
-        for (int t = 0; t < 6; ++t) {
-            float4 r; r.x = row[4*t+0]; r.y = row[4*t+1]; r.z = row[4*t+2]; r.w = row[4*t+3];
-            vp[t] = r;
+        if (v0) {
+            const float sa = sabuf[e0];
+            const int pos = posbuf[e0];
+            float row[24];
+#pragma unroll
+            for (int o = 0; o < 8; ++o)
+#pragma unroll
+                for (int c = 0; c < 3; ++c)
+                    row[o*3+c] = sa * (T30[o]*sh_v0[c] + R0[o*3+c]) * sc;
+            float4* vp = (float4*)(vbuf + (size_t)pos * 40 + 16);
+#pragma unroll
+            for (int t = 0; t < 6; ++t) {
+                float4 r; r.x = row[4*t+0]; r.y = row[4*t+1]; r.z = row[4*t+2]; r.w = row[4*t+3];
+                vp[t] = r;
+            }
+        }
+        if (v1) {
+            const float sa = sabuf[e1];
+            const int pos = posbuf[e1];
+            float row[24];
+#pragma unroll
+            for (int o = 0; o < 8; ++o)
+#pragma unroll
+                for (int c = 0; c < 3; ++c)
+                    row[o*3+c] = sa * (T31[o]*sh_v1[c] + R1[o*3+c]) * sc;
+            float4* vp = (float4*)(vbuf + (size_t)pos * 40 + 16);
+#pragma unroll
+            for (int t = 0; t < 6; ++t) {
+                float4 r; r.x = row[4*t+0]; r.y = row[4*t+1]; r.z = row[4*t+2]; r.w = row[4*t+3];
+                vp[t] = r;
+            }
         }
     }
 }
```

Result: slower. 525.9 us (+77.4%).
